# Kernel optimization log

Measured on AMD Instinct MI355X. Metric: run time of the kernel, lower is better.

## Reference

```python
import jax, jax.numpy as jnp
import numpy as np

NGRID = 40
NTOKEN = NGRID * NGRID          # 1600
FEAT = 128
DK = 64
HEAD = 8
NLAYER = 4
EPS = 1e-5
DXDY = (1.0 / (NGRID - 1)) ** 2
SDK = 1.0 / np.sqrt(DK)


def _edges():
    g = jnp.linspace(0.0, 1.0, NGRID)
    gx, gy = jnp.meshgrid(g, g, indexing='ij')
    grid = jnp.stack([gx, gy], axis=-1).reshape(NTOKEN, 2)          # (T,2)
    gi = jnp.broadcast_to(grid[:, None, :], (NTOKEN, NTOKEN, 2))
    gj = jnp.broadcast_to(grid[None, :, :], (NTOKEN, NTOKEN, 2))
    return jnp.concatenate([gi, gj], axis=-1).reshape(NTOKEN * NTOKEN, 4)


def _mlp(x, W1, b1, W2, b2, W3, b3):
    # DenseNet([4,32,64,1], LeakyReLU): activation between layers, none after last
    h = jax.nn.leaky_relu(x @ W1 + b1)
    h = jax.nn.leaky_relu(h @ W2 + b2)
    return h @ W3 + b3


def setup_inputs() -> dict:
    key = jax.random.key(0)
    ks = jax.random.split(key, 24)
    d = {}
    d['xy'] = jax.random.normal(ks[0], (8, 2 * NTOKEN, FEAT), dtype=jnp.float32)
    # kernel / kernelf DenseNet params [4,32,64,1]
    def lin(k, fi, fo):
        s = 1.0 / np.sqrt(fi)
        k1, k2 = jax.random.split(k)
        return (jax.random.uniform(k1, (fi, fo), jnp.float32, -s, s),
                jax.random.uniform(k2, (fo,), jnp.float32, -s, s))
    d['kW1'], d['kb1'] = lin(ks[1], 4, 32)
    d['kW2'], d['kb2'] = lin(ks[2], 32, 64)
    d['kW3'], d['kb3'] = lin(ks[3], 64, 1)
    d['fW1'], d['fb1'] = lin(ks[4], 4, 32)
    d['fW2'], d['fb2'] = lin(ks[5], 32, 64)
    d['fW3'], d['fb3'] = lin(ks[6], 64, 1)
    s = 1.0 / np.sqrt(FEAT)
    d['Wq'] = jax.random.uniform(ks[7], (NLAYER, HEAD, FEAT, DK), jnp.float32, -s, s)
    d['bq'] = jax.random.uniform(ks[8], (NLAYER, HEAD, DK), jnp.float32, -s, s)
    d['Wk'] = jax.random.uniform(ks[9], (NLAYER, HEAD, FEAT, DK), jnp.float32, -s, s)
    d['bk'] = jax.random.uniform(ks[10], (NLAYER, HEAD, DK), jnp.float32, -s, s)
    d['g0'] = jnp.ones((2 * NTOKEN, FEAT), jnp.float32)
    d['b0'] = jnp.zeros((2 * NTOKEN, FEAT), jnp.float32)
    d['gl'] = jnp.ones((NLAYER - 1, FEAT), jnp.float32)
    d['bl'] = jnp.zeros((NLAYER - 1, FEAT), jnp.float32)
    return d


def reference(xy, kW1, kb1, kW2, kb2, kW3, kb3, fW1, fb1, fW2, fb2, fW3, fb3,
              Wq, bq, Wk, bk, g0, b0, gl, bl):
    edges = _edges()                                                   # (T*T,4)
    weight = _mlp(edges, kW1, kb1, kW2, kb2, kW3, kb3).reshape(NTOKEN, NTOKEN)
    weightf = _mlp(edges, fW1, fb1, fW2, fb2, fW3, fb3).reshape(NTOKEN, NTOKEN)
    W2 = jnp.concatenate([weight, weightf], axis=-1)                   # (T, 2T)

    # fcn[0]: LayerNorm over last two dims [2T, F]
    mu = jnp.mean(xy, axis=(1, 2), keepdims=True)
    var = jnp.var(xy, axis=(1, 2), keepdims=True)
    V = (xy - mu) * jax.lax.rsqrt(var + EPS) * g0 + b0                 # (B,2T,F)

    scale = DXDY * SDK
    for j in range(NLAYER - 1):
        Q = jnp.einsum('btf,hfd->bhtd', V, Wq[j]) + bq[j][None, :, None, :]
        K = jnp.einsum('btf,hfd->bhtd', V, Wk[j]) + bk[j][None, :, None, :]
        KV = jnp.einsum('bhtd,btf->bhdf', K, V) * scale                # (B,H,dk,F)
        mid = jnp.einsum('bhtd,bhdf->btf', Q, KV)                      # sum over heads
        m = jnp.mean(mid, axis=-1, keepdims=True)
        v = jnp.var(mid, axis=-1, keepdims=True)
        V = (mid - m) * jax.lax.rsqrt(v + EPS) * gl[j] + bl[j] + V

    j = NLAYER - 1
    Q = jnp.einsum('btf,hfd->bhtd', V, Wq[j]) + bq[j][None, :, None, :]
    K = jnp.einsum('btf,hfd->bhtd', V, Wk[j]) + bk[j][None, :, None, :]
    KV = jnp.einsum('bhtd,btf->bhdf', K[:, :, :NTOKEN, :], xy[:, :NTOKEN, :]) * scale
    out = DXDY * jnp.einsum('nm,bhmd,bhdf->bnf', W2, Q, KV)            # (B,T,F)
    return out
```

## Files before the change

### kernel.cpp

```cpp
#include <hip/hip_runtime.h>
#include <math.h>

#define NGRID 40
#define NT    1600
#define T2    3200
#define F     128
#define NB    8
#define EPS   1e-5f

__device__ __constant__ const float kINV39 = 1.0f/39.0f;
constexpr float DXDY  = (1.0f/39.0f)*(1.0f/39.0f);
constexpr float SCALE = DXDY * 0.125f;

typedef __attribute__((ext_vector_type(8))) short bf16x8;
typedef __attribute__((ext_vector_type(4))) float f32x4;
typedef __attribute__((ext_vector_type(4))) unsigned uint4v;

__device__ __forceinline__ unsigned bitu(float f){ return __builtin_bit_cast(unsigned,f); }
__device__ __forceinline__ float bitf(unsigned u){ return __builtin_bit_cast(float,u); }
__device__ __forceinline__ unsigned short f2bf(float f) {
    unsigned u = bitu(f);
    unsigned r = u + 0x7FFFu + ((u >> 16) & 1u);
    return (unsigned short)(r >> 16);
}
__device__ __forceinline__ float bf2f(unsigned short h) { return bitf(((unsigned)h) << 16); }

__device__ __forceinline__ void pack_hl(float a, float b, unsigned &h, unsigned &l) {
    unsigned ua = bitu(a), ub = bitu(b);
    h = __builtin_amdgcn_perm(ub, ua, 0x07060302u);
    float ra = a - bitf(ua & 0xffff0000u);
    float rb = b - bitf(ub & 0xffff0000u);
    l = __builtin_amdgcn_perm(bitu(rb), bitu(ra), 0x07060302u);
}
__device__ __forceinline__ void store8u(short* dst, const unsigned* p) {
    uint4v v0 = {p[0], p[1], p[2], p[3]};
    uint4v v1 = {p[4], p[5], p[6], p[7]};
    *(uint4v*)dst = v0;
    *(uint4v*)(dst + 8) = v1;
}
__device__ __forceinline__ void store16u(short* dst, const unsigned* p) {
    store8u(dst, p);
    store8u(dst + 16, p + 8);
}

__global__ __launch_bounds__(512) void k_prep_frag(
    const float* __restrict__ kW2, const float* __restrict__ fW2,
    short* __restrict__ Ah, short* __restrict__ Al)
{
    int tid = threadIdx.x;
    int wid = tid >> 6, lane = tid & 63;
    int mlp = wid >> 2, oc = wid & 3;
    const float* W2 = mlp ? fW2 : kW2;
    int row = lane & 15;
    int k0 = (lane >> 4) * 8;
    #pragma unroll
    for (int i = 0; i < 8; ++i) {
        float w = W2[(size_t)(k0 + i) * 64 + oc * 16 + row];
        unsigned short h = f2bf(w);
        Ah[((mlp*4 + oc)*64 + lane)*8 + i] = (short)h;
        Al[((mlp*4 + oc)*64 + lane)*8 + i] = (short)f2bf(w - bf2f(h));
    }
}

__global__ __launch_bounds__(256) void k_prep_uv(
    const float* __restrict__ kW1, const float* __restrict__ kb1,
    const float* __restrict__ fW1, const float* __restrict__ fb1,
    float* __restrict__ uv)
{
    int idx = blockIdx.x * 256 + threadIdx.x;
    int node = idx >> 5, o = idx & 31;
    float x0 = (float)(node / NGRID) * kINV39;
    float x1 = (float)(node % NGRID) * kINV39;
    uv[idx]          = fmaf(kW1[o], x0, fmaf(kW1[32+o], x1, kb1[o]));
    uv[51200 + idx]  = fmaf(kW1[64+o], x0, kW1[96+o]*x1);
    uv[102400 + idx] = fmaf(fW1[o], x0, fmaf(fW1[32+o], x1, fb1[o]));
    uv[153600 + idx] = fmaf(fW1[64+o], x0, fW1[96+o]*x1);
}

#define MLPGRID 1536
__global__ __launch_bounds__(256, 2) void k_mlp_mfma(
    const float* __restrict__ uv,
    const float* __restrict__ kb2, const float* __restrict__ kW3,
    const float* __restrict__ kb3,
    const float* __restrict__ fb2, const float* __restrict__ fW3,
    const float* __restrict__ fb3,
    const short* __restrict__ Ah, const short* __restrict__ Al,
    short* __restrict__ W2h)
{
    int tid = threadIdx.x;
    int wid = tid >> 6, lane = tid & 63;
    int c = lane & 15, kg = lane >> 4;
    int k0 = kg * 8;

    bf16x8 AHf[2][4], ALf[2][4];
    float4 B2f[2][4], W3f[2][4];
    #pragma unroll
    for (int mlp = 0; mlp < 2; ++mlp) {
        const float* b2p = mlp ? fb2 : kb2;
        const float* w3p = mlp ? fW3 : kW3;
        #pragma unroll
        for (int oc = 0; oc < 4; ++oc) {
            AHf[mlp][oc] = *(const bf16x8*)&Ah[((mlp*4 + oc)*64 + lane)*8];
            ALf[mlp][oc] = *(const bf16x8*)&Al[((mlp*4 + oc)*64 + lane)*8];
            B2f[mlp][oc] = *(const float4*)&b2p[oc*16 + kg*4];
            W3f[mlp][oc] = *(const float4*)&w3p[oc*16 + kg*4];
        }
    }
    float bias0 = kb3[0], bias1 = fb3[0];

    int tile = blockIdx.x*4 + wid;
    int n = tile / 100;
    int mt = tile - n*100;
    while (tile < 160000) {
        int m = mt*16 + c;
        float res0, res1;
        #pragma unroll
        for (int mlp = 0; mlp < 2; ++mlp) {
            const float* up = uv + mlp*102400 + n*32 + k0;
            const float* vp = uv + mlp*102400 + 51200 + m*32 + k0;
            float4 ua = *(const float4*)up;
            float4 ub = *(const float4*)(up + 4);
            float4 va = *(const float4*)vp;
            float4 vb = *(const float4*)(vp + 4);
            float h[8] = {ua.x+va.x, ua.y+va.y, ua.z+va.z, ua.w+va.w,
                          ub.x+vb.x, ub.y+vb.y, ub.z+vb.z, ub.w+vb.w};
            #pragma unroll
            for (int i = 0; i < 8; ++i) h[i] = fmaxf(h[i], 0.01f*h[i]);
            unsigned bhp[4], blp[4];
            #pragma unroll
            for (int p = 0; p < 4; ++p)
                pack_hl(h[2*p], h[2*p+1], bhp[p], blp[p]);
            uint4v bhv = {bhp[0], bhp[1], bhp[2], bhp[3]};
            uint4v blv = {blp[0], blp[1], blp[2], blp[3]};
            bf16x8 bh = __builtin_bit_cast(bf16x8, bhv);
            bf16x8 bl = __builtin_bit_cast(bf16x8, blv);
            float acc = 0.f;
            #pragma unroll
            for (int oc = 0; oc < 4; ++oc) {
                f32x4 d = {B2f[mlp][oc].x, B2f[mlp][oc].y,
                           B2f[mlp][oc].z, B2f[mlp][oc].w};
                d = __builtin_amdgcn_mfma_f32_16x16x32_bf16(AHf[mlp][oc], bh, d, 0, 0, 0);
                d = __builtin_amdgcn_mfma_f32_16x16x32_bf16(ALf[mlp][oc], bh, d, 0, 0, 0);
                d = __builtin_amdgcn_mfma_f32_16x16x32_bf16(AHf[mlp][oc], bl, d, 0, 0, 0);
                float w3v[4] = {W3f[mlp][oc].x, W3f[mlp][oc].y,
                                W3f[mlp][oc].z, W3f[mlp][oc].w};
                #pragma unroll
                for (int r = 0; r < 4; ++r)
                    acc = fmaf(fmaxf(d[r], 0.01f*d[r]), w3v[r], acc);
            }
            if (mlp == 0) res0 = acc; else res1 = acc;
        }
        res0 += __shfl_xor(res0, 16); res0 += __shfl_xor(res0, 32);
        res1 += __shfl_xor(res1, 16); res1 += __shfl_xor(res1, 32);
        if (lane < 16) {
            W2h[(size_t)n*T2 + m]      = (short)f2bf(res0 + bias0);
            W2h[(size_t)n*T2 + NT + m] = (short)f2bf(res1 + bias1);
        }
        tile += MLPGRID*4;
        n += 61; mt += 44;
        if (mt >= 100) { mt -= 100; ++n; }
    }
}

__global__ __launch_bounds__(256) void k_precompute_P(
    const float* __restrict__ Wq, const float* __restrict__ bq,
    const float* __restrict__ Wk, const float* __restrict__ bk,
    short* __restrict__ Pnh, short* __restrict__ Pnl,
    float* __restrict__ uB, float* __restrict__ wB, float* __restrict__ cB)
{
    int j = blockIdx.x;
    int part = blockIdx.y;
    const float* wq = Wq + (size_t)j*8*F*64;
    const float* wk = Wk + (size_t)j*8*F*64;
    int tid = threadIdx.x;
    if (part == 8) {
        const float* bqj = bq + j*512;
        const float* bkj = bk + j*512;
        if (tid < 128) {
            int k = tid; float a = 0.f;
            for (int h = 0; h < 8; ++h)
                for (int d = 0; d < 64; ++d)
                    a = fmaf(wq[((size_t)h*F + k)*64 + d], bkj[h*64 + d], a);
            uB[j*128 + k] = a;
        } else {
            int k = tid - 128; float a = 0.f;
            for (int h = 0; h < 8; ++h)
                for (int d = 0; d < 64; ++d)
                    a = fmaf(wk[((size_t)h*F + k)*64 + d], bqj[h*64 + d], a);
            wB[j*128 + k] = a;
        }
        if (tid == 0) {
            float a = 0.f;
            for (int i = 0; i < 512; ++i) a = fmaf(bqj[i], bkj[i], a);
            cB[j] = a;
        }
        return;
    }
    int kp = part*16 + (tid >> 4);
    int k0 = (tid & 15) * 8;
    float acc[8] = {0,0,0,0,0,0,0,0};
    for (int h = 0; h < 8; ++h) {
        const float* wkrow = wk + ((size_t)h*F + kp)*64;
        for (int d = 0; d < 64; ++d) {
            float bv = wkrow[d];
            #pragma unroll
            for (int i = 0; i < 8; ++i)
                acc[i] = fmaf(wq[((size_t)h*F + k0 + i)*64 + d], bv, acc[i]);
        }
    }
    #pragma unroll
    for (int i = 0; i < 8; ++i) {
        float val = acc[i];
        short hs = (short)(bitu(val) >> 16);
        float rem = val - bitf(bitu(val) & 0xffff0000u);
        short ls = (short)(bitu(rem) >> 16);
        Pnh[((size_t)j*128 + k0 + i)*128 + kp] = hs;
        Pnl[((size_t)j*128 + k0 + i)*128 + kp] = ls;
    }
}

__global__ __launch_bounds__(256) void k_ln0_part(
    const float* __restrict__ xy, float* __restrict__ part)
{
    int b = blockIdx.x, blk = blockIdx.y;
    const float4* p = (const float4*)xy + (size_t)b*102400 + blk*4096 + threadIdx.x;
    float s = 0.f, q = 0.f;
    #pragma unroll
    for (int i = 0; i < 16; ++i) {
        float4 v = p[i*256];
        s += (v.x + v.y) + (v.z + v.w);
        q += (v.x*v.x + v.y*v.y) + (v.z*v.z + v.w*v.w);
    }
    #pragma unroll
    for (int off = 32; off >= 1; off >>= 1) {
        s += __shfl_xor(s, off);
        q += __shfl_xor(q, off);
    }
    __shared__ float ss[4], qs[4];
    int wid = threadIdx.x >> 6;
    if ((threadIdx.x & 63) == 0) { ss[wid] = s; qs[wid] = q; }
    __syncthreads();
    if (threadIdx.x == 0) {
        part[((size_t)b*25 + blk)*2 + 0] = ss[0]+ss[1]+ss[2]+ss[3];
        part[((size_t)b*25 + blk)*2 + 1] = qs[0]+qs[1]+qs[2]+qs[3];
    }
}

__global__ void k_ln0_stats(const float* __restrict__ part, float* __restrict__ stats)
{
    int b = threadIdx.x;
    if (b < NB) {
        float s = 0.f, q = 0.f;
        for (int i = 0; i < 25; ++i) {
            s += part[((size_t)b*25 + i)*2 + 0];
            q += part[((size_t)b*25 + i)*2 + 1];
        }
        float mu  = s * (1.0f/409600.0f);
        float var = q * (1.0f/409600.0f) - mu*mu;
        stats[b*2 + 0] = mu;
        stats[b*2 + 1] = rsqrtf(var + EPS);
    }
}

__global__ __launch_bounds__(256) void k_ln0_apply(
    const float* __restrict__ xy, const float* __restrict__ g0,
    const float* __restrict__ b0, const float* __restrict__ stats,
    short* __restrict__ Vbh, short* __restrict__ Vbl,
    short* __restrict__ Vbth, short* __restrict__ Vbtl,
    float* __restrict__ spartV)
{
    int tgrp = blockIdx.x, b = blockIdx.y;
    float mu = stats[b*2], rs = stats[b*2+1];
    __shared__ float T[64][132];
    int tid = threadIdx.x;
    int r = tid >> 2, q = tid & 3;
    int f2 = tid >> 1, half = tid & 1;
    #pragma unroll
    for (int p = 0; p < 2; ++p) {
        int t0 = tgrp*128 + p*64;
        {
            int t = t0 + r;
            const float* xp = xy + ((size_t)b*T2 + t)*F + q*32;
            const float* gp = g0 + (size_t)t*F + q*32;
            const float* bp = b0 + (size_t)t*F + q*32;
            unsigned ph[16], pl[16];
            #pragma unroll
            for (int i = 0; i < 32; i += 4) {
                float4 x = *(const float4*)&xp[i];
                float4 g = *(const float4*)&gp[i];
                float4 bb = *(const float4*)&bp[i];
                float o0 = (x.x - mu)*rs*g.x + bb.x;
                float o1 = (x.y - mu)*rs*g.y + bb.y;
                float o2 = (x.z - mu)*rs*g.z + bb.z;
                float o3 = (x.w - mu)*rs*g.w + bb.w;
                T[r][q*32+i] = o0; T[r][q*32+i+1] = o1;
                T[r][q*32+i+2] = o2; T[r][q*32+i+3] = o3;
                pack_hl(o0, o1, ph[i>>1], pl[i>>1]);
                pack_hl(o2, o3, ph[(i>>1)+1], pl[(i>>1)+1]);
            }
            size_t ob = ((size_t)b*T2 + t)*F + q*32;
            store16u(&Vbh[ob], ph);
            store16u(&Vbl[ob], pl);
        }
        __syncthreads();
        {
            float sacc = 0.f;
            unsigned ph[16], pl[16];
            #pragma unroll
            for (int i = 0; i < 32; i += 2) {
                float v0 = T[half*32 + i][f2];
                float v1 = T[half*32 + i + 1][f2];
                sacc += v0 + v1;
                pack_hl(v0, v1, ph[i>>1], pl[i>>1]);
            }
            size_t ob = ((size_t)b*F + f2)*T2 + t0 + half*32;
            store16u(&Vbth[ob], ph);
            store16u(&Vbtl[ob], pl);
            spartV[((size_t)b*100 + (tgrp*2+p)*2 + half)*128 + f2] = sacc;
        }
        __syncthreads();
    }
}

__global__ __launch_bounds__(256) void k_prep_xyt(
    const float* __restrict__ xy,
    short* __restrict__ xyTh, short* __restrict__ xyTl,
    float* __restrict__ s2part)
{
    int tgrp = blockIdx.x, b = blockIdx.y;
    __shared__ float T[64][132];
    int tid = threadIdx.x;
    int r = tid >> 2, q = tid & 3;
    int f2 = tid >> 1, half = tid & 1;
    int t0 = tgrp*64;
    {
        const float* xp = xy + ((size_t)b*T2 + t0 + r)*F + q*32;
        #pragma unroll
        for (int i = 0; i < 32; i += 4)
            *(float4*)&T[r][q*32+i] = *(const float4*)&xp[i];
    }
    __syncthreads();
    {
        float sacc = 0.f;
        unsigned ph[16], pl[16];
        #pragma unroll
        for (int i = 0; i < 32; i += 2) {
            float v0 = T[half*32 + i][f2];
            float v1 = T[half*32 + i + 1][f2];
            sacc += v0 + v1;
            pack_hl(v0, v1, ph[i>>1], pl[i>>1]);
        }
        size_t ob = ((size_t)b*F + f2)*1600 + t0 + half*32;
        store16u(&xyTh[ob], ph);
        store16u(&xyTl[ob], pl);
        s2part[((size_t)b*50 + tgrp*2 + half)*128 + f2] = sacc;
    }
}

__global__ __launch_bounds__(256) void k_gemm_g_sym(
    const short* __restrict__ Xh, const short* __restrict__ Xl,
    float* __restrict__ Gpart)
{
    int split = blockIdx.x, b = blockIdx.y;
    int t0 = split*128;
    __shared__ __align__(16) short Sh[2][128][40], Sl[2][128][40];
    int tid = threadIdx.x;
    int lane = tid & 63, wid = tid >> 6;
    int wr = wid >> 1, wc = wid & 1;
    int r16 = lane & 15, kg = lane >> 4;
    int sf = tid >> 1, th = tid & 1;

    const short* ph_ = Xh + ((size_t)b*F + sf)*T2 + t0 + th*16;
    const short* pl_ = Xl + ((size_t)b*F + sf)*T2 + t0 + th*16;

    f32x4 acc[4][4];
    #pragma unroll
    for (int i = 0; i < 4; ++i)
        #pragma unroll
        for (int j2 = 0; j2 < 4; ++j2)
            acc[i][j2] = (f32x4){0.f,0.f,0.f,0.f};

    {
        uint4v h0 = *(const uint4v*)ph_,      h1 = *(const uint4v*)(ph_ + 8);
        uint4v l0 = *(const uint4v*)pl_,      l1 = *(const uint4v*)(pl_ + 8);
        *(uint4v*)&Sh[0][sf][th*16]     = h0; *(uint4v*)&Sh[0][sf][th*16+8] = h1;
        *(uint4v*)&Sl[0][sf][th*16]     = l0; *(uint4v*)&Sl[0][sf][th*16+8] = l1;
    }
    #pragma unroll
    for (int ks = 0; ks < 4; ++ks) {
        int cur = ks & 1;
        uint4v h0, h1, l0, l1;
        if (ks < 3) {
            int ko = (ks+1)*32;
            h0 = *(const uint4v*)(ph_ + ko); h1 = *(const uint4v*)(ph_ + ko + 8);
            l0 = *(const uint4v*)(pl_ + ko); l1 = *(const uint4v*)(pl_ + ko + 8);
        }
        __syncthreads();
        bf16x8 ah[4], al[4], bh[4], bl[4];
        #pragma unroll
        for (int i = 0; i < 4; ++i) {
            ah[i] = *(const bf16x8*)&Sh[cur][wr*64 + i*16 + r16][kg*8];
            al[i] = *(const bf16x8*)&Sl[cur][wr*64 + i*16 + r16][kg*8];
            bh[i] = *(const bf16x8*)&Sh[cur][wc*64 + i*16 + r16][kg*8];
            bl[i] = *(const bf16x8*)&Sl[cur][wc*64 + i*16 + r16][kg*8];
        }
        #pragma unroll
        for (int i = 0; i < 4; ++i)
            #pragma unroll
            for (int j2 = 0; j2 < 4; ++j2) {
                acc[i][j2] = __builtin_amdgcn_mfma_f32_16x16x32_bf16(ah[i], bh[j2], acc[i][j2], 0,0,0);
                acc[i][j2] = __builtin_amdgcn_mfma_f32_16x16x32_bf16(al[i], bh[j2], acc[i][j2], 0,0,0);
                acc[i][j2] = __builtin_amdgcn_mfma_f32_16x16x32_bf16(ah[i], bl[j2], acc[i][j2], 0,0,0);
            }
        if (ks < 3) {
            int nb = cur ^ 1;
            *(uint4v*)&Sh[nb][sf][th*16]     = h0; *(uint4v*)&Sh[nb][sf][th*16+8] = h1;
            *(uint4v*)&Sl[nb][sf][th*16]     = l0; *(uint4v*)&Sl[nb][sf][th*16+8] = l1;
        }
    }
    size_t gb = ((size_t)b*25 + split)*16384;
    #pragma unroll
    for (int i = 0; i < 4; ++i)
        #pragma unroll
        for (int j2 = 0; j2 < 4; ++j2)
            #pragma unroll
            for (int reg = 0; reg < 4; ++reg)
                Gpart[gb + (size_t)(wr*64 + i*16 + kg*4 + reg)*128 + wc*64 + j2*16 + r16]
                    = acc[i][j2][reg];
}

__global__ __launch_bounds__(256) void k_gemm_g_asym(
    const short* __restrict__ Ah_, const short* __restrict__ Al_,
    const short* __restrict__ Bh_, const short* __restrict__ Bl_,
    float* __restrict__ Gpart)
{
    int split = blockIdx.x, b = blockIdx.y;
    int t0 = split*64;
    __shared__ __align__(16) short Ahs[128][40], Als[128][40], Bhs[128][40], Bls[128][40];
    int tid = threadIdx.x;
    int lane = tid & 63, wid = tid >> 6;
    int wr = wid >> 1, wc = wid & 1;
    int r16 = lane & 15, kg = lane >> 4;
    int sf = tid >> 1, th = tid & 1;

    const short* pah = Ah_ + ((size_t)b*F + sf)*1600 + t0 + th*16;
    const short* pal = Al_ + ((size_t)b*F + sf)*1600 + t0 + th*16;
    const short* pbh = Bh_ + ((size_t)b*F + sf)*T2   + t0 + th*16;
    const short* pbl = Bl_ + ((size_t)b*F + sf)*T2   + t0 + th*16;

    f32x4 acc[4][4];
    #pragma unroll
    for (int i = 0; i < 4; ++i)
        #pragma unroll
        for (int j2 = 0; j2 < 4; ++j2)
            acc[i][j2] = (f32x4){0.f,0.f,0.f,0.f};

    #pragma unroll
    for (int ks = 0; ks < 2; ++ks) {
        int ko = ks*32;
        if (ks) __syncthreads();
        *(uint4v*)&Ahs[sf][th*16]   = *(const uint4v*)(pah + ko);
        *(uint4v*)&Ahs[sf][th*16+8] = *(const uint4v*)(pah + ko + 8);
        *(uint4v*)&Als[sf][th*16]   = *(const uint4v*)(pal + ko);
        *(uint4v*)&Als[sf][th*16+8] = *(const uint4v*)(pal + ko + 8);
        *(uint4v*)&Bhs[sf][th*16]   = *(const uint4v*)(pbh + ko);
        *(uint4v*)&Bhs[sf][th*16+8] = *(const uint4v*)(pbh + ko + 8);
        *(uint4v*)&Bls[sf][th*16]   = *(const uint4v*)(pbl + ko);
        *(uint4v*)&Bls[sf][th*16+8] = *(const uint4v*)(pbl + ko + 8);
        __syncthreads();
        bf16x8 ah[4], al[4], bh[4], bl[4];
        #pragma unroll
        for (int i = 0; i < 4; ++i) {
            ah[i] = *(const bf16x8*)&Ahs[wr*64 + i*16 + r16][kg*8];
            al[i] = *(const bf16x8*)&Als[wr*64 + i*16 + r16][kg*8];
            bh[i] = *(const bf16x8*)&Bhs[wc*64 + i*16 + r16][kg*8];
            bl[i] = *(const bf16x8*)&Bls[wc*64 + i*16 + r16][kg*8];
        }
        #pragma unroll
        for (int i = 0; i < 4; ++i)
            #pragma unroll
            for (int j2 = 0; j2 < 4; ++j2) {
                acc[i][j2] = __builtin_amdgcn_mfma_f32_16x16x32_bf16(ah[i], bh[j2], acc[i][j2], 0,0,0);
                acc[i][j2] = __builtin_amdgcn_mfma_f32_16x16x32_bf16(al[i], bh[j2], acc[i][j2], 0,0,0);
                acc[i][j2] = __builtin_amdgcn_mfma_f32_16x16x32_bf16(ah[i], bl[j2], acc[i][j2], 0,0,0);
            }
    }
    size_t gb = ((size_t)b*25 + split)*16384;
    #pragma unroll
    for (int i = 0; i < 4; ++i)
        #pragma unroll
        for (int j2 = 0; j2 < 4; ++j2)
            #pragma unroll
            for (int reg = 0; reg < 4; ++reg)
                Gpart[gb + (size_t)(wr*64 + i*16 + kg*4 + reg)*128 + wc*64 + j2*16 + r16]
                    = acc[i][j2][reg];
}

__global__ __launch_bounds__(256) void k_gred(
    const float* __restrict__ Gpart, const float* __restrict__ wj,
    short* __restrict__ Gbh, short* __restrict__ Gbl, float* __restrict__ rpart)
{
    int part = blockIdx.x, b = blockIdx.y;
    int tid = threadIdx.x;
    int e0 = part*2048 + tid*8;
    float a[8] = {0,0,0,0,0,0,0,0};
    for (int i = 0; i < 25; ++i) {
        const float* p = Gpart + ((size_t)b*25 + i)*16384 + e0;
        float4 x0 = *(const float4*)p;
        float4 x1 = *(const float4*)(p + 4);
        a[0] += x0.x; a[1] += x0.y; a[2] += x0.z; a[3] += x0.w;
        a[4] += x1.x; a[5] += x1.y; a[6] += x1.z; a[7] += x1.w;
    }
    unsigned ph[4], pl[4];
    #pragma unroll
    for (int i = 0; i < 8; i += 2) pack_hl(a[i], a[i+1], ph[i>>1], pl[i>>1]);
    uint4v vh = {ph[0],ph[1],ph[2],ph[3]};
    uint4v vl = {pl[0],pl[1],pl[2],pl[3]};
    *(uint4v*)&Gbh[(size_t)b*16384 + e0] = vh;
    *(uint4v*)&Gbl[(size_t)b*16384 + e0] = vl;

    int c0 = e0 & 127;
    float4 w0 = *(const float4*)&wj[c0];
    float4 w1 = *(const float4*)&wj[c0 + 4];
    float pr = a[0]*w0.x + a[1]*w0.y + a[2]*w0.z + a[3]*w0.w
             + a[4]*w1.x + a[5]*w1.y + a[6]*w1.z + a[7]*w1.w;
    pr += __shfl_xor(pr, 1); pr += __shfl_xor(pr, 2);
    pr += __shfl_xor(pr, 4); pr += __shfl_xor(pr, 8);
    if ((tid & 15) == 0) rpart[b*128 + (e0 >> 7)] = pr;
}

struct CMStage {
    short Psh[2][64][40], Psl[2][64][40];
    short Bsh[2][128][40], Bsl[2][128][40];
};
__global__ __launch_bounds__(256) void k_computeM(
    const short* __restrict__ Gbh, const short* __restrict__ Gbl,
    const float* __restrict__ spart, int np,
    const short* __restrict__ Pjh, const short* __restrict__ Pjl,
    const float* __restrict__ uj, const float* __restrict__ cj,
    const float* __restrict__ rpart,
    short* __restrict__ Mth, short* __restrict__ Mtl, float* __restrict__ rm)
{
    int kh = blockIdx.x, b = blockIdx.y;
    __shared__ __align__(16) char smem[sizeof(CMStage)];
    CMStage& S = *(CMStage*)smem;
    float (*T)[132] = (float(*)[132])smem;
    __shared__ float sv[128];

    int tid = threadIdx.x;
    int lane = tid & 63, wid = tid >> 6;
    int wr = wid >> 1, wc = wid & 1;
    int r16 = lane & 15, kg = lane >> 4;
    int st = tid >> 2, sq = tid & 3;
    int sf = tid >> 1, sh2 = tid & 1;

    if (tid < 128) {
        float s = 0.f;
        for (int i = 0; i < np; ++i) s += spart[((size_t)b*np + i)*128 + tid];
        sv[tid] = s;
        if (kh == 0) rm[b*128 + tid] = SCALE*(rpart[b*128 + tid] + cj[0]*s);
    }

    const short* pah = Pjh + (size_t)(kh*64 + st)*128 + sq*8;
    const short* pal = Pjl + (size_t)(kh*64 + st)*128 + sq*8;
    const short* pbh = Gbh + ((size_t)b*F + sf)*128 + sh2*16;
    const short* pbl = Gbl + ((size_t)b*F + sf)*128 + sh2*16;

    f32x4 acc[2][4];
    #pragma unroll
    for (int i = 0; i < 2; ++i)
        #pragma unroll
        for (int j2 = 0; j2 < 4; ++j2)
            acc[i][j2] = (f32x4){0.f,0.f,0.f,0.f};

    {
        *(uint4v*)&S.Psh[0][st][sq*8]      = *(const uint4v*)pah;
        *(uint4v*)&S.Psl[0][st][sq*8]      = *(const uint4v*)pal;
        *(uint4v*)&S.Bsh[0][sf][sh2*16]    = *(const uint4v*)pbh;
        *(uint4v*)&S.Bsh[0][sf][sh2*16+8]  = *(const uint4v*)(pbh + 8);
        *(uint4v*)&S.Bsl[0][sf][sh2*16]    = *(const uint4v*)pbl;
        *(uint4v*)&S.Bsl[0][sf][sh2*16+8]  = *(const uint4v*)(pbl + 8);
    }
    #pragma unroll
    for (int ks = 0; ks < 4; ++ks) {
        int cur = ks & 1;
        uint4v a0, a1, b0, b1, b2, b3;
        if (ks < 3) {
            int ko = (ks+1)*32;
            a0 = *(const uint4v*)(pah + ko); a1 = *(const uint4v*)(pal + ko);
            b0 = *(const uint4v*)(pbh + ko); b1 = *(const uint4v*)(pbh + ko + 8);
            b2 = *(const uint4v*)(pbl + ko); b3 = *(const uint4v*)(pbl + ko + 8);
        }
        __syncthreads();
        bf16x8 ah[2], al[2], bh[4], bl[4];
        #pragma unroll
        for (int i = 0; i < 2; ++i) {
            ah[i] = *(const bf16x8*)&S.Psh[cur][wr*32 + i*16 + r16][kg*8];
            al[i] = *(const bf16x8*)&S.Psl[cur][wr*32 + i*16 + r16][kg*8];
        }
        #pragma unroll
        for (int j2 = 0; j2 < 4; ++j2) {
            bh[j2] = *(const bf16x8*)&S.Bsh[cur][wc*64 + j2*16 + r16][kg*8];
            bl[j2] = *(const bf16x8*)&S.Bsl[cur][wc*64 + j2*16 + r16][kg*8];
        }
        #pragma unroll
        for (int i = 0; i < 2; ++i)
            #pragma unroll
            for (int j2 = 0; j2 < 4; ++j2) {
                acc[i][j2] = __builtin_amdgcn_mfma_f32_16x16x32_bf16(ah[i], bh[j2], acc[i][j2], 0,0,0);
                acc[i][j2] = __builtin_amdgcn_mfma_f32_16x16x32_bf16(al[i], bh[j2], acc[i][j2], 0,0,0);
                acc[i][j2] = __builtin_amdgcn_mfma_f32_16x16x32_bf16(ah[i], bl[j2], acc[i][j2], 0,0,0);
            }
        if (ks < 3) {
            int nb = cur ^ 1;
            *(uint4v*)&S.Psh[nb][st][sq*8]     = a0;
            *(uint4v*)&S.Psl[nb][st][sq*8]     = a1;
            *(uint4v*)&S.Bsh[nb][sf][sh2*16]   = b0;
            *(uint4v*)&S.Bsh[nb][sf][sh2*16+8] = b1;
            *(uint4v*)&S.Bsl[nb][sf][sh2*16]   = b2;
            *(uint4v*)&S.Bsl[nb][sf][sh2*16+8] = b3;
        }
    }
    float uval[2][4], svv[4];
    #pragma unroll
    for (int i = 0; i < 2; ++i)
        #pragma unroll
        for (int reg = 0; reg < 4; ++reg)
            uval[i][reg] = uj[kh*64 + wr*32 + i*16 + kg*4 + reg];
    #pragma unroll
    for (int j2 = 0; j2 < 4; ++j2) svv[j2] = sv[wc*64 + j2*16 + r16];
    __syncthreads();
    #pragma unroll
    for (int i = 0; i < 2; ++i)
        #pragma unroll
        for (int j2 = 0; j2 < 4; ++j2)
            #pragma unroll
            for (int reg = 0; reg < 4; ++reg)
                T[wr*32 + i*16 + kg*4 + reg][wc*64 + j2*16 + r16]
                    = SCALE*(acc[i][j2][reg] + uval[i][reg]*svv[j2]);
    __syncthreads();
    {
        int f2 = tid >> 1, half = tid & 1;
        unsigned ph[16], pl[16];
        #pragma unroll
        for (int i = 0; i < 32; i += 2) {
            float v0 = T[half*32 + i][f2];
            float v1 = T[half*32 + i + 1][f2];
            pack_hl(v0, v1, ph[i>>1], pl[i>>1]);
        }
        size_t ob = ((size_t)b*F + f2)*F + kh*64 + half*32;
        store16u(&Mth[ob], ph);
        store16u(&Mtl[ob], pl);
    }
}

struct MidStage {
    short Ash[2][64][40], Asl[2][64][40];
    short Bsh[2][128][40], Bsl[2][128][40];
};
__global__ __launch_bounds__(256) void k_mid(
    short* __restrict__ Vbh, short* __restrict__ Vbl,
    const short* __restrict__ Mth, const short* __restrict__ Mtl,
    const float* __restrict__ rm,
    const float* __restrict__ glj, const float* __restrict__ blj, int doLN,
    short* __restrict__ OTh, short* __restrict__ OTl,
    float* __restrict__ spartN)
{
    int tblk = blockIdx.x, b = blockIdx.y;
    int t0 = tblk * 64;
    __shared__ __align__(16) char smem[sizeof(MidStage)];
    MidStage& S = *(MidStage*)smem;
    float (*T)[132] = (float(*)[132])smem;

    int tid = threadIdx.x;
    int lane = tid & 63, wid = tid >> 6;
    int wr = wid >> 1, wc = wid & 1;
    int r16 = lane & 15, kg = lane >> 4;
    int st = tid >> 2, sq = tid & 3;
    int sf = tid >> 1, sh2 = tid & 1;

    const short* pah = Vbh + ((size_t)b*T2 + t0 + st)*F + sq*8;
    const short* pal = Vbl + ((size_t)b*T2 + t0 + st)*F + sq*8;
    const short* pbh = Mth + ((size_t)b*F + sf)*F + sh2*16;
    const short* pbl = Mtl + ((size_t)b*F + sf)*F + sh2*16;

    f32x4 acc[2][4];
    #pragma unroll
    for (int i = 0; i < 2; ++i)
        #pragma unroll
        for (int j2 = 0; j2 < 4; ++j2)
            acc[i][j2] = (f32x4){0.f,0.f,0.f,0.f};

    {
        *(uint4v*)&S.Ash[0][st][sq*8]      = *(const uint4v*)pah;
        *(uint4v*)&S.Asl[0][st][sq*8]      = *(const uint4v*)pal;
        *(uint4v*)&S.Bsh[0][sf][sh2*16]    = *(const uint4v*)pbh;
        *(uint4v*)&S.Bsh[0][sf][sh2*16+8]  = *(const uint4v*)(pbh + 8);
        *(uint4v*)&S.Bsl[0][sf][sh2*16]    = *(const uint4v*)pbl;
        *(uint4v*)&S.Bsl[0][sf][sh2*16+8]  = *(const uint4v*)(pbl + 8);
    }
    #pragma unroll
    for (int ks = 0; ks < 4; ++ks) {
        int cur = ks & 1;
        uint4v a0, a1, b0, b1, b2, b3;
        if (ks < 3) {
            int ko = (ks+1)*32;
            a0 = *(const uint4v*)(pah + ko); a1 = *(const uint4v*)(pal + ko);
            b0 = *(const uint4v*)(pbh + ko); b1 = *(const uint4v*)(pbh + ko + 8);
            b2 = *(const uint4v*)(pbl + ko); b3 = *(const uint4v*)(pbl + ko + 8);
        }
        __syncthreads();
        bf16x8 ah[2], al[2], bh[4], bl[4];
        #pragma unroll
        for (int i = 0; i < 2; ++i) {
            ah[i] = *(const bf16x8*)&S.Ash[cur][wr*32 + i*16 + r16][kg*8];
            al[i] = *(const bf16x8*)&S.Asl[cur][wr*32 + i*16 + r16][kg*8];
        }
        #pragma unroll
        for (int j2 = 0; j2 < 4; ++j2) {
            bh[j2] = *(const bf16x8*)&S.Bsh[cur][wc*64 + j2*16 + r16][kg*8];
            bl[j2] = *(const bf16x8*)&S.Bsl[cur][wc*64 + j2*16 + r16][kg*8];
        }
        #pragma unroll
        for (int i = 0; i < 2; ++i)
            #pragma unroll
            for (int j2 = 0; j2 < 4; ++j2) {
                acc[i][j2] = __builtin_amdgcn_mfma_f32_16x16x32_bf16(ah[i], bh[j2], acc[i][j2], 0,0,0);
                acc[i][j2] = __builtin_amdgcn_mfma_f32_16x16x32_bf16(al[i], bh[j2], acc[i][j2], 0,0,0);
                acc[i][j2] = __builtin_amdgcn_mfma_f32_16x16x32_bf16(ah[i], bl[j2], acc[i][j2], 0,0,0);
            }
        if (ks < 3) {
            int nb = cur ^ 1;
            *(uint4v*)&S.Ash[nb][st][sq*8]     = a0;
            *(uint4v*)&S.Asl[nb][st][sq*8]     = a1;
            *(uint4v*)&S.Bsh[nb][sf][sh2*16]   = b0;
            *(uint4v*)&S.Bsh[nb][sf][sh2*16+8] = b1;
            *(uint4v*)&S.Bsl[nb][sf][sh2*16]   = b2;
            *(uint4v*)&S.Bsl[nb][sf][sh2*16+8] = b3;
        }
    }
    float rv[4];
    #pragma unroll
    for (int j2 = 0; j2 < 4; ++j2) rv[j2] = rm[b*F + wc*64 + j2*16 + r16];
    __syncthreads();
    #pragma unroll
    for (int i = 0; i < 2; ++i)
        #pragma unroll
        for (int j2 = 0; j2 < 4; ++j2)
            #pragma unroll
            for (int reg = 0; reg < 4; ++reg)
                T[wr*32 + i*16 + kg*4 + reg][wc*64 + j2*16 + r16]
                    = acc[i][j2][reg] + rv[j2];
    __syncthreads();

    if (doLN) {
        int r = tid >> 2, q = tid & 3;
        float v[32];
        #pragma unroll
        for (int i = 0; i < 32; i += 4)
            *(float4*)&v[i] = *(const float4*)&T[r][q*32 + i];
        float s = 0.f;
        #pragma unroll
        for (int i = 0; i < 32; ++i) s += v[i];
        s += __shfl_xor(s, 1); s += __shfl_xor(s, 2);
        float mu = s * (1.0f/128.0f);
        float dv = 0.f;
        #pragma unroll
        for (int i = 0; i < 32; ++i) { float d = v[i] - mu; dv = fmaf(d, d, dv); }
        dv += __shfl_xor(dv, 1); dv += __shfl_xor(dv, 2);
        float rs = rsqrtf(dv * (1.0f/128.0f) + EPS);

        short hb[32], lb[32];
        {
            const short* rh = Vbh + ((size_t)b*T2 + t0 + r)*F + q*32;
            const short* rl = Vbl + ((size_t)b*T2 + t0 + r)*F + q*32;
            #pragma unroll
            for (int i = 0; i < 32; i += 8) {
                *(uint4v*)&hb[i] = *(const uint4v*)(rh + i);
                *(uint4v*)&lb[i] = *(const uint4v*)(rl + i);
            }
        }
        float gv[32], bv2[32];
        #pragma unroll
        for (int i = 0; i < 32; i += 4) {
            *(float4*)&gv[i]  = *(const float4*)&glj[q*32 + i];
            *(float4*)&bv2[i] = *(const float4*)&blj[q*32 + i];
        }
        unsigned ph[16], pl[16];
        #pragma unroll
        for (int i = 0; i < 32; i += 2) {
            float res0 = bf2f((unsigned short)hb[i])   + bf2f((unsigned short)lb[i]);
            float res1 = bf2f((unsigned short)hb[i+1]) + bf2f((unsigned short)lb[i+1]);
            float o0 = (v[i]   - mu)*rs*gv[i]   + bv2[i]   + res0;
            float o1 = (v[i+1] - mu)*rs*gv[i+1] + bv2[i+1] + res1;
            T[r][q*32+i] = o0; T[r][q*32+i+1] = o1;
            pack_hl(o0, o1, ph[i>>1], pl[i>>1]);
        }
        size_t ob = ((size_t)b*T2 + t0 + r)*F + q*32;
        store16u(&Vbh[ob], ph);
        store16u(&Vbl[ob], pl);
        __syncthreads();
    }
    {
        int f2 = tid >> 1, half = tid & 1;
        float sacc = 0.f;
        unsigned ph[16], pl[16];
        #pragma unroll
        for (int i = 0; i < 32; i += 2) {
            float v0 = T[half*32 + i][f2];
            float v1 = T[half*32 + i + 1][f2];
            sacc += v0 + v1;
            pack_hl(v0, v1, ph[i>>1], pl[i>>1]);
        }
        size_t ob = ((size_t)b*F + f2)*T2 + t0 + half*32;
        store16u(&OTh[ob], ph);
        store16u(&OTl[ob], pl);
        if (doLN)
            spartN[((size_t)b*100 + tblk*2 + half)*128 + f2] = sacc;
    }
}

__global__ __launch_bounds__(256) void k_gemm_out_mfma(
    const short* __restrict__ W2h,
    const short* __restrict__ Uth, const short* __restrict__ Utl,
    float* __restrict__ out)
{
    int id = blockIdx.x;
    int qb = id >> 3;
    if (qb >= 25) return;
    int job = (id & 7) * 25 + qb;
    int nt = job >> 3, b = job & 7;
    int n0 = nt * 64;

    __shared__ __align__(16) short As[2][64][40];
    __shared__ __align__(16) short Bh_s[2][128][40], Bl_s[2][128][40];

    int tid = threadIdx.x;
    int lane = tid & 63, wid = tid >> 6;
    int wr = wid >> 1, wc = wid & 1;
    int r16 = lane & 15, kg = lane >> 4;
    int srow = tid >> 2, sq2 = tid & 3;
    int sf = tid >> 1, sh2 = tid & 1;

    const short* ap  = W2h + (size_t)(n0 + srow)*T2 + sq2*8;
    const short* bhp = Uth + ((size_t)b*F + sf)*T2 + sh2*16;
    const short* blp = Utl + ((size_t)b*F + sf)*T2 + sh2*16;

    f32x4 acc[2][4];
    #pragma unroll
    for (int i = 0; i < 2; ++i)
        #pragma unroll
        for (int j2 = 0; j2 < 4; ++j2)
            acc[i][j2] = (f32x4){0.f,0.f,0.f,0.f};

    {
        *(uint4v*)&As[0][srow][sq2*8]     = *(const uint4v*)ap;
        *(uint4v*)&Bh_s[0][sf][sh2*16]    = *(const uint4v*)bhp;
        *(uint4v*)&Bh_s[0][sf][sh2*16+8]  = *(const uint4v*)(bhp + 8);
        *(uint4v*)&Bl_s[0][sf][sh2*16]    = *(const uint4v*)blp;
        *(uint4v*)&Bl_s[0][sf][sh2*16+8]  = *(const uint4v*)(blp + 8);
    }
    for (int it = 0; it < 100; ++it) {
        int cur = it & 1;
        uint4v ra, b0, b1, b2, b3;
        if (it < 99) {
            int ko = (it + 1) * 32;
            ra = *(const uint4v*)(ap + ko);
            b0 = *(const uint4v*)(bhp + ko); b1 = *(const uint4v*)(bhp + ko + 8);
            b2 = *(const uint4v*)(blp + ko); b3 = *(const uint4v*)(blp + ko + 8);
        }
        __syncthreads();
        bf16x8 ah[2], bh[4], bl[4];
        #pragma unroll
        for (int i = 0; i < 2; ++i)
            ah[i] = *(const bf16x8*)&As[cur][wr*32 + i*16 + r16][kg*8];
        #pragma unroll
        for (int j2 = 0; j2 < 4; ++j2) {
            bh[j2] = *(const bf16x8*)&Bh_s[cur][wc*64 + j2*16 + r16][kg*8];
            bl[j2] = *(const bf16x8*)&Bl_s[cur][wc*64 + j2*16 + r16][kg*8];
        }
        #pragma unroll
        for (int i = 0; i < 2; ++i)
            #pragma unroll
            for (int j2 = 0; j2 < 4; ++j2) {
                acc[i][j2] = __builtin_amdgcn_mfma_f32_16x16x32_bf16(ah[i], bh[j2], acc[i][j2], 0,0,0);
                acc[i][j2] = __builtin_amdgcn_mfma_f32_16x16x32_bf16(ah[i], bl[j2], acc[i][j2], 0,0,0);
            }
        if (it < 99) {
            int nb = cur ^ 1;
            *(uint4v*)&As[nb][srow][sq2*8]    = ra;
            *(uint4v*)&Bh_s[nb][sf][sh2*16]   = b0;
            *(uint4v*)&Bh_s[nb][sf][sh2*16+8] = b1;
            *(uint4v*)&Bl_s[nb][sf][sh2*16]   = b2;
            *(uint4v*)&Bl_s[nb][sf][sh2*16+8] = b3;
        }
    }
    #pragma unroll
    for (int i = 0; i < 2; ++i)
        #pragma unroll
        for (int j2 = 0; j2 < 4; ++j2)
            #pragma unroll
            for (int reg = 0; reg < 4; ++reg) {
                int n_out = n0 + wr*32 + i*16 + kg*4 + reg;
                int f_out = wc*64 + j2*16 + r16;
                out[((size_t)b*NT + n_out)*F + f_out] = DXDY * acc[i][j2][reg];
            }
}

extern "C" void kernel_launch(void* const* d_in, const int* in_sizes, int n_in,
                              void* d_out, int out_size, void* d_ws, size_t ws_size,
                              hipStream_t stream)
{
    const float* xy  = (const float*)d_in[0];
    const float* kW1 = (const float*)d_in[1];
    const float* kb1 = (const float*)d_in[2];
    const float* kW2 = (const float*)d_in[3];
    const float* kb2 = (const float*)d_in[4];
    const float* kW3 = (const float*)d_in[5];
    const float* kb3 = (const float*)d_in[6];
    const float* fW1 = (const float*)d_in[7];
    const float* fb1 = (const float*)d_in[8];
    const float* fW2 = (const float*)d_in[9];
    const float* fb2 = (const float*)d_in[10];
    const float* fW3 = (const float*)d_in[11];
    const float* fb3 = (const float*)d_in[12];
    const float* Wq  = (const float*)d_in[13];
    const float* bq  = (const float*)d_in[14];
    const float* Wk  = (const float*)d_in[15];
    const float* bk  = (const float*)d_in[16];
    const float* g0  = (const float*)d_in[17];
    const float* b0  = (const float*)d_in[18];
    const float* gl  = (const float*)d_in[19];
    const float* bl  = (const float*)d_in[20];
    float* out = (float*)d_out;

    short* W2h  = (short*)d_ws;
    short* Vbh  = W2h  + 5120000;
    short* Vbl  = Vbh  + 3276800;
    short* Vbth = Vbl  + 3276800;
    short* Vbtl = Vbth + 3276800;
    short* xyTh = Vbtl + 3276800;
    short* xyTl = xyTh + 1638400;
    short* Uth  = xyTl + 1638400;
    short* Utl  = Uth  + 3276800;
    short* Pnh  = Utl  + 3276800;
    short* Pnl  = Pnh  + 65536;
    short* Mth  = Pnl  + 65536;
    short* Mtl  = Mth  + 131072;
    short* Gbh  = Mtl  + 131072;
    short* Gbl  = Gbh  + 131072;
    short* AhF  = Gbl  + 131072;
    short* AlF  = AhF  + 4096;
    float* Gpart  = (float*)(AlF + 4096);
    float* uB     = Gpart + 3276800;
    float* wB     = uB + 512;
    float* cB     = wB + 512;
    float* lnpart = cB + 4;
    float* lnstats= lnpart + 400;
    float* rpart  = lnstats + 16;
    float* rm     = rpart + 1024;
    float* spartV = rm + 1024;
    float* s2part = spartV + 102400;
    float* uvT    = s2part + 51200;

    k_prep_frag<<<1, 512, 0, stream>>>(kW2, fW2, AhF, AlF);
    k_prep_uv<<<dim3(200), 256, 0, stream>>>(kW1, kb1, fW1, fb1, uvT);
    k_mlp_mfma<<<dim3(MLPGRID), 256, 0, stream>>>(uvT, kb2, kW3, kb3,
                                                  fb2, fW3, fb3, AhF, AlF, W2h);
    k_precompute_P<<<dim3(4,9), 256, 0, stream>>>(Wq, bq, Wk, bk, Pnh, Pnl, uB, wB, cB);
    k_ln0_part<<<dim3(8,25), 256, 0, stream>>>(xy, lnpart);
    k_ln0_stats<<<1, 64, 0, stream>>>(lnpart, lnstats);
    k_ln0_apply<<<dim3(25,8), 256, 0, stream>>>(xy, g0, b0, lnstats,
                                                Vbh, Vbl, Vbth, Vbtl, spartV);
    k_prep_xyt<<<dim3(25,8), 256, 0, stream>>>(xy, xyTh, xyTl, s2part);

    for (int j = 0; j < 4; ++j) {
        if (j < 3)
            k_gemm_g_sym<<<dim3(25,8), 256, 0, stream>>>(Vbth, Vbtl, Gpart);
        else
            k_gemm_g_asym<<<dim3(25,8), 256, 0, stream>>>(xyTh, xyTl, Vbth, Vbtl, Gpart);
        k_gred<<<dim3(8,8), 256, 0, stream>>>(Gpart, wB + j*128, Gbh, Gbl, rpart);
        k_computeM<<<dim3(2,8), 256, 0, stream>>>(
            Gbh, Gbl,
            (j < 3) ? spartV : s2part, (j < 3) ? 100 : 50,
            Pnh + (size_t)j*16384, Pnl + (size_t)j*16384,
            uB + j*128, cB + j, rpart, Mth, Mtl, rm);
        if (j < 3)
            k_mid<<<dim3(50,8), 256, 0, stream>>>(Vbh, Vbl, Mth, Mtl, rm,
                                                  gl + j*128, bl + j*128, 1,
                                                  Vbth, Vbtl, spartV);
        else
            k_mid<<<dim3(50,8), 256, 0, stream>>>(Vbh, Vbl, Mth, Mtl, rm,
                                                  gl, bl, 0,
                                                  Uth, Utl, spartV);
    }

    k_gemm_out_mfma<<<dim3(256), 256, 0, stream>>>(W2h, Uth, Utl, out);
}
```

Baseline: 548.5 us.

## Merge prep kernels and run layer loop as one cooperative persistent kernel

Several small setup kernels (uv prep, LN partial sums, P precompute, W2 fragment prep) are merged into one launch, and the LN stats kernel is removed by having each apply block reduce the partials itself. The whole per-layer chain (gemm G, reduce, computeM, mid, final output GEMM) now runs inside a single cooperative kernel that uses grid.sync between stages, removing about twenty kernel launches and their gaps. If the cooperative launch fails, the code falls back to separate wrapper kernels. The cost is grid-wide barriers with many blocks idle in the small stages, a shared-memory union sized for the largest stage, and the output GEMM now running on 200 blocks instead of 256.

```diff
diff --git a/kernel.cpp b/kernel.cpp
--- a/kernel.cpp
+++ b/kernel.cpp
@@ -1,5 +1,8 @@
 #include <hip/hip_runtime.h>
+#include <hip/hip_cooperative_groups.h>
 #include <math.h>
+
+namespace cg = cooperative_groups;
 
 #define NGRID 40
 #define NT    1600
@@ -43,38 +46,124 @@
     store8u(dst + 16, p + 8);
 }
 
-__global__ __launch_bounds__(512) void k_prep_frag(
+__global__ __launch_bounds__(256) void k_prep(
     const float* __restrict__ kW2, const float* __restrict__ fW2,
-    short* __restrict__ Ah, short* __restrict__ Al)
-{
-    int tid = threadIdx.x;
-    int wid = tid >> 6, lane = tid & 63;
-    int mlp = wid >> 2, oc = wid & 3;
-    const float* W2 = mlp ? fW2 : kW2;
-    int row = lane & 15;
-    int k0 = (lane >> 4) * 8;
-    #pragma unroll
-    for (int i = 0; i < 8; ++i) {
-        float w = W2[(size_t)(k0 + i) * 64 + oc * 16 + row];
-        unsigned short h = f2bf(w);
-        Ah[((mlp*4 + oc)*64 + lane)*8 + i] = (short)h;
-        Al[((mlp*4 + oc)*64 + lane)*8 + i] = (short)f2bf(w - bf2f(h));
-    }
-}
-
-__global__ __launch_bounds__(256) void k_prep_uv(
+    short* __restrict__ Ah, short* __restrict__ Al,
     const float* __restrict__ kW1, const float* __restrict__ kb1,
     const float* __restrict__ fW1, const float* __restrict__ fb1,
-    float* __restrict__ uv)
-{
-    int idx = blockIdx.x * 256 + threadIdx.x;
-    int node = idx >> 5, o = idx & 31;
-    float x0 = (float)(node / NGRID) * kINV39;
-    float x1 = (float)(node % NGRID) * kINV39;
-    uv[idx]          = fmaf(kW1[o], x0, fmaf(kW1[32+o], x1, kb1[o]));
-    uv[51200 + idx]  = fmaf(kW1[64+o], x0, kW1[96+o]*x1);
-    uv[102400 + idx] = fmaf(fW1[o], x0, fmaf(fW1[32+o], x1, fb1[o]));
-    uv[153600 + idx] = fmaf(fW1[64+o], x0, fW1[96+o]*x1);
+    float* __restrict__ uv,
+    const float* __restrict__ xy, float* __restrict__ lnpart,
+    const float* __restrict__ Wq, const float* __restrict__ bq,
+    const float* __restrict__ Wk, const float* __restrict__ bk,
+    short* __restrict__ Pnh, short* __restrict__ Pnl,
+    float* __restrict__ uB, float* __restrict__ wB, float* __restrict__ cB)
+{
+    __shared__ float ss[4], qs[4];
+    int job = blockIdx.x;
+    int tid = threadIdx.x;
+    if (job < 200) {
+        int idx = job * 256 + tid;
+        int node = idx >> 5, o = idx & 31;
+        float x0 = (float)(node / NGRID) * kINV39;
+        float x1 = (float)(node % NGRID) * kINV39;
+        uv[idx]          = fmaf(kW1[o], x0, fmaf(kW1[32+o], x1, kb1[o]));
+        uv[51200 + idx]  = fmaf(kW1[64+o], x0, kW1[96+o]*x1);
+        uv[102400 + idx] = fmaf(fW1[o], x0, fmaf(fW1[32+o], x1, fb1[o]));
+        uv[153600 + idx] = fmaf(fW1[64+o], x0, fW1[96+o]*x1);
+        return;
+    }
+    if (job < 400) {
+        int t = job - 200;
+        int b = t & 7, blk = t >> 3;
+        const float4* p = (const float4*)xy + (size_t)b*102400 + blk*4096 + tid;
+        float s = 0.f, q = 0.f;
+        #pragma unroll
+        for (int i = 0; i < 16; ++i) {
+            float4 v = p[i*256];
+            s += (v.x + v.y) + (v.z + v.w);
+            q += (v.x*v.x + v.y*v.y) + (v.z*v.z + v.w*v.w);
+        }
+        #pragma unroll
+        for (int off = 32; off >= 1; off >>= 1) {
+            s += __shfl_xor(s, off);
+            q += __shfl_xor(q, off);
+        }
+        int wid = tid >> 6;
+        if ((tid & 63) == 0) { ss[wid] = s; qs[wid] = q; }
+        __syncthreads();
+        if (tid == 0) {
+            lnpart[((size_t)b*25 + blk)*2 + 0] = ss[0]+ss[1]+ss[2]+ss[3];
+            lnpart[((size_t)b*25 + blk)*2 + 1] = qs[0]+qs[1]+qs[2]+qs[3];
+        }
+        return;
+    }
+    if (job < 436) {
+        int t = job - 400;
+        int j = t & 3, part = t >> 2;
+        const float* wq = Wq + (size_t)j*8*F*64;
+        const float* wk = Wk + (size_t)j*8*F*64;
+        if (part == 8) {
+            const float* bqj = bq + j*512;
+            const float* bkj = bk + j*512;
+            if (tid < 128) {
+                int k = tid; float a = 0.f;
+                for (int h = 0; h < 8; ++h)
+                    for (int d = 0; d < 64; ++d)
+                        a = fmaf(wq[((size_t)h*F + k)*64 + d], bkj[h*64 + d], a);
+                uB[j*128 + k] = a;
+            } else {
+                int k = tid - 128; float a = 0.f;
+                for (int h = 0; h < 8; ++h)
+                    for (int d = 0; d < 64; ++d)
+                        a = fmaf(wk[((size_t)h*F + k)*64 + d], bqj[h*64 + d], a);
+                wB[j*128 + k] = a;
+            }
+            if (tid == 0) {
+                float a = 0.f;
+                for (int i = 0; i < 512; ++i) a = fmaf(bqj[i], bkj[i], a);
+                cB[j] = a;
+            }
+            return;
+        }
+        int kp = part*16 + (tid >> 4);
+        int k0 = (tid & 15) * 8;
+        float acc[8] = {0,0,0,0,0,0,0,0};
+        for (int h = 0; h < 8; ++h) {
+            const float* wkrow = wk + ((size_t)h*F + kp)*64;
+            for (int d = 0; d < 64; ++d) {
+                float bv = wkrow[d];
+                #pragma unroll
+                for (int i = 0; i < 8; ++i)
+                    acc[i] = fmaf(wq[((size_t)h*F + k0 + i)*64 + d], bv, acc[i]);
+            }
+        }
+        #pragma unroll
+        for (int i = 0; i < 8; ++i) {
+            float val = acc[i];
+            short hs = (short)(bitu(val) >> 16);
+            float rem = val - bitf(bitu(val) & 0xffff0000u);
+            short ls = (short)(bitu(rem) >> 16);
+            Pnh[((size_t)j*128 + k0 + i)*128 + kp] = hs;
+            Pnl[((size_t)j*128 + k0 + i)*128 + kp] = ls;
+        }
+        return;
+    }
+    {
+        int oc = tid >> 6, lane = tid & 63;
+        int row = lane & 15;
+        int k0 = (lane >> 4) * 8;
+        #pragma unroll
+        for (int mlp = 0; mlp < 2; ++mlp) {
+            const float* W2 = mlp ? fW2 : kW2;
+            #pragma unroll
+            for (int i = 0; i < 8; ++i) {
+                float w = W2[(size_t)(k0 + i) * 64 + oc * 16 + row];
+                unsigned short h = f2bf(w);
+                Ah[((mlp*4 + oc)*64 + lane)*8 + i] = (short)h;
+                Al[((mlp*4 + oc)*64 + lane)*8 + i] = (short)f2bf(w - bf2f(h));
+            }
+        }
+    }
 }
 
 #define MLPGRID 1536
@@ -162,127 +251,43 @@
     }
 }
 
-__global__ __launch_bounds__(256) void k_precompute_P(
-    const float* __restrict__ Wq, const float* __restrict__ bq,
-    const float* __restrict__ Wk, const float* __restrict__ bk,
-    short* __restrict__ Pnh, short* __restrict__ Pnl,
-    float* __restrict__ uB, float* __restrict__ wB, float* __restrict__ cB)
-{
-    int j = blockIdx.x;
-    int part = blockIdx.y;
-    const float* wq = Wq + (size_t)j*8*F*64;
-    const float* wk = Wk + (size_t)j*8*F*64;
-    int tid = threadIdx.x;
-    if (part == 8) {
-        const float* bqj = bq + j*512;
-        const float* bkj = bk + j*512;
-        if (tid < 128) {
-            int k = tid; float a = 0.f;
-            for (int h = 0; h < 8; ++h)
-                for (int d = 0; d < 64; ++d)
-                    a = fmaf(wq[((size_t)h*F + k)*64 + d], bkj[h*64 + d], a);
-            uB[j*128 + k] = a;
-        } else {
-            int k = tid - 128; float a = 0.f;
-            for (int h = 0; h < 8; ++h)
-                for (int d = 0; d < 64; ++d)
-                    a = fmaf(wk[((size_t)h*F + k)*64 + d], bqj[h*64 + d], a);
-            wB[j*128 + k] = a;
-        }
-        if (tid == 0) {
-            float a = 0.f;
-            for (int i = 0; i < 512; ++i) a = fmaf(bqj[i], bkj[i], a);
-            cB[j] = a;
-        }
-        return;
-    }
-    int kp = part*16 + (tid >> 4);
-    int k0 = (tid & 15) * 8;
-    float acc[8] = {0,0,0,0,0,0,0,0};
-    for (int h = 0; h < 8; ++h) {
-        const float* wkrow = wk + ((size_t)h*F + kp)*64;
-        for (int d = 0; d < 64; ++d) {
-            float bv = wkrow[d];
-            #pragma unroll
-            for (int i = 0; i < 8; ++i)
-                acc[i] = fmaf(wq[((size_t)h*F + k0 + i)*64 + d], bv, acc[i]);
-        }
-    }
-    #pragma unroll
-    for (int i = 0; i < 8; ++i) {
-        float val = acc[i];
-        short hs = (short)(bitu(val) >> 16);
-        float rem = val - bitf(bitu(val) & 0xffff0000u);
-        short ls = (short)(bitu(rem) >> 16);
-        Pnh[((size_t)j*128 + k0 + i)*128 + kp] = hs;
-        Pnl[((size_t)j*128 + k0 + i)*128 + kp] = ls;
-    }
-}
-
-__global__ __launch_bounds__(256) void k_ln0_part(
-    const float* __restrict__ xy, float* __restrict__ part)
-{
-    int b = blockIdx.x, blk = blockIdx.y;
-    const float4* p = (const float4*)xy + (size_t)b*102400 + blk*4096 + threadIdx.x;
-    float s = 0.f, q = 0.f;
-    #pragma unroll
-    for (int i = 0; i < 16; ++i) {
-        float4 v = p[i*256];
-        s += (v.x + v.y) + (v.z + v.w);
-        q += (v.x*v.x + v.y*v.y) + (v.z*v.z + v.w*v.w);
-    }
-    #pragma unroll
-    for (int off = 32; off >= 1; off >>= 1) {
-        s += __shfl_xor(s, off);
-        q += __shfl_xor(q, off);
-    }
-    __shared__ float ss[4], qs[4];
-    int wid = threadIdx.x >> 6;
-    if ((threadIdx.x & 63) == 0) { ss[wid] = s; qs[wid] = q; }
-    __syncthreads();
-    if (threadIdx.x == 0) {
-        part[((size_t)b*25 + blk)*2 + 0] = ss[0]+ss[1]+ss[2]+ss[3];
-        part[((size_t)b*25 + blk)*2 + 1] = qs[0]+qs[1]+qs[2]+qs[3];
-    }
-}
-
-__global__ void k_ln0_stats(const float* __restrict__ part, float* __restrict__ stats)
-{
-    int b = threadIdx.x;
-    if (b < NB) {
-        float s = 0.f, q = 0.f;
-        for (int i = 0; i < 25; ++i) {
-            s += part[((size_t)b*25 + i)*2 + 0];
-            q += part[((size_t)b*25 + i)*2 + 1];
-        }
-        float mu  = s * (1.0f/409600.0f);
-        float var = q * (1.0f/409600.0f) - mu*mu;
-        stats[b*2 + 0] = mu;
-        stats[b*2 + 1] = rsqrtf(var + EPS);
-    }
-}
-
-__global__ __launch_bounds__(256) void k_ln0_apply(
+struct SMem {
+    __align__(16) char buf[61440];
+    float sv[128];
+};
+struct GSymS  { short Sh[2][128][40], Sl[2][128][40]; };
+struct GAsymS { short Ahs[128][40], Als[128][40], Bhs[128][40], Bls[128][40]; };
+struct CMS    { short Psh[2][64][40], Psl[2][64][40], Bsh[2][128][40], Bsl[2][128][40]; };
+struct MidS   { short Ash[2][64][40], Asl[2][64][40], Bsh[2][128][40], Bsl[2][128][40]; };
+struct GOutS  { short As[2][64][40], Bh[2][128][40], Bl[2][128][40]; };
+
+__device__ void body_apply(int job,
     const float* __restrict__ xy, const float* __restrict__ g0,
-    const float* __restrict__ b0, const float* __restrict__ stats,
+    const float* __restrict__ b0, const float* __restrict__ lnpart,
     short* __restrict__ Vbh, short* __restrict__ Vbl,
     short* __restrict__ Vbth, short* __restrict__ Vbtl,
-    float* __restrict__ spartV)
-{
-    int tgrp = blockIdx.x, b = blockIdx.y;
-    float mu = stats[b*2], rs = stats[b*2+1];
-    __shared__ float T[64][132];
+    float* __restrict__ spartV, SMem& S)
+{
+    int tgrp = job % 25, b = job / 25;
+    float s = 0.f, q = 0.f;
+    for (int i = 0; i < 25; ++i) {
+        s += lnpart[((size_t)b*25 + i)*2 + 0];
+        q += lnpart[((size_t)b*25 + i)*2 + 1];
+    }
+    float mu = s * (1.0f/409600.0f);
+    float rs = rsqrtf(q * (1.0f/409600.0f) - mu*mu + EPS);
+    float (*T)[132] = (float(*)[132])S.buf;
     int tid = threadIdx.x;
-    int r = tid >> 2, q = tid & 3;
+    int r = tid >> 2, qd = tid & 3;
     int f2 = tid >> 1, half = tid & 1;
     #pragma unroll
     for (int p = 0; p < 2; ++p) {
         int t0 = tgrp*128 + p*64;
         {
             int t = t0 + r;
-            const float* xp = xy + ((size_t)b*T2 + t)*F + q*32;
-            const float* gp = g0 + (size_t)t*F + q*32;
-            const float* bp = b0 + (size_t)t*F + q*32;
+            const float* xp = xy + ((size_t)b*T2 + t)*F + qd*32;
+            const float* gp = g0 + (size_t)t*F + qd*32;
+            const float* bp = b0 + (size_t)t*F + qd*32;
             unsigned ph[16], pl[16];
             #pragma unroll
             for (int i = 0; i < 32; i += 4) {
@@ -293,12 +298,12 @@
                 float o1 = (x.y - mu)*rs*g.y + bb.y;
                 float o2 = (x.z - mu)*rs*g.z + bb.z;
                 float o3 = (x.w - mu)*rs*g.w + bb.w;
-                T[r][q*32+i] = o0; T[r][q*32+i+1] = o1;
-                T[r][q*32+i+2] = o2; T[r][q*32+i+3] = o3;
+                T[r][qd*32+i] = o0; T[r][qd*32+i+1] = o1;
+                T[r][qd*32+i+2] = o2; T[r][qd*32+i+3] = o3;
                 pack_hl(o0, o1, ph[i>>1], pl[i>>1]);
                 pack_hl(o2, o3, ph[(i>>1)+1], pl[(i>>1)+1]);
             }
-            size_t ob = ((size_t)b*T2 + t)*F + q*32;
+            size_t ob = ((size_t)b*T2 + t)*F + qd*32;
             store16u(&Vbh[ob], ph);
             store16u(&Vbl[ob], pl);
         }
@@ -322,22 +327,22 @@
     }
 }
 
-__global__ __launch_bounds__(256) void k_prep_xyt(
+__device__ void body_xyt(int job,
     const float* __restrict__ xy,
     short* __restrict__ xyTh, short* __restrict__ xyTl,
-    float* __restrict__ s2part)
-{
-    int tgrp = blockIdx.x, b = blockIdx.y;
-    __shared__ float T[64][132];
+    float* __restrict__ s2part, SMem& S)
+{
+    int tgrp = job % 25, b = job / 25;
+    float (*T)[132] = (float(*)[132])S.buf;
     int tid = threadIdx.x;
-    int r = tid >> 2, q = tid & 3;
+    int r = tid >> 2, qd = tid & 3;
     int f2 = tid >> 1, half = tid & 1;
     int t0 = tgrp*64;
     {
-        const float* xp = xy + ((size_t)b*T2 + t0 + r)*F + q*32;
+        const float* xp = xy + ((size_t)b*T2 + t0 + r)*F + qd*32;
         #pragma unroll
         for (int i = 0; i < 32; i += 4)
-            *(float4*)&T[r][q*32+i] = *(const float4*)&xp[i];
+            *(float4*)&T[r][qd*32+i] = *(const float4*)&xp[i];
     }
     __syncthreads();
     {
@@ -357,13 +362,13 @@
     }
 }
 
-__global__ __launch_bounds__(256) void k_gemm_g_sym(
+__device__ void body_gsym(int job,
     const short* __restrict__ Xh, const short* __restrict__ Xl,
-    float* __restrict__ Gpart)
-{
-    int split = blockIdx.x, b = blockIdx.y;
+    float* __restrict__ Gpart, SMem& Smem)
+{
+    int split = job % 25, b = job / 25;
     int t0 = split*128;
-    __shared__ __align__(16) short Sh[2][128][40], Sl[2][128][40];
+    GSymS& S = *(GSymS*)Smem.buf;
     int tid = threadIdx.x;
     int lane = tid & 63, wid = tid >> 6;
     int wr = wid >> 1, wc = wid & 1;
@@ -383,8 +388,8 @@
     {
         uint4v h0 = *(const uint4v*)ph_,      h1 = *(const uint4v*)(ph_ + 8);
         uint4v l0 = *(const uint4v*)pl_,      l1 = *(const uint4v*)(pl_ + 8);
-        *(uint4v*)&Sh[0][sf][th*16]     = h0; *(uint4v*)&Sh[0][sf][th*16+8] = h1;
-        *(uint4v*)&Sl[0][sf][th*16]     = l0; *(uint4v*)&Sl[0][sf][th*16+8] = l1;
+        *(uint4v*)&S.Sh[0][sf][th*16]     = h0; *(uint4v*)&S.Sh[0][sf][th*16+8] = h1;
+        *(uint4v*)&S.Sl[0][sf][th*16]     = l0; *(uint4v*)&S.Sl[0][sf][th*16+8] = l1;
     }
     #pragma unroll
     for (int ks = 0; ks < 4; ++ks) {
@@ -399,10 +404,10 @@
         bf16x8 ah[4], al[4], bh[4], bl[4];
         #pragma unroll
         for (int i = 0; i < 4; ++i) {
-            ah[i] = *(const bf16x8*)&Sh[cur][wr*64 + i*16 + r16][kg*8];
-            al[i] = *(const bf16x8*)&Sl[cur][wr*64 + i*16 + r16][kg*8];
-            bh[i] = *(const bf16x8*)&Sh[cur][wc*64 + i*16 + r16][kg*8];
-            bl[i] = *(const bf16x8*)&Sl[cur][wc*64 + i*16 + r16][kg*8];
+            ah[i] = *(const bf16x8*)&S.Sh[cur][wr*64 + i*16 + r16][kg*8];
+            al[i] = *(const bf16x8*)&S.Sl[cur][wr*64 + i*16 + r16][kg*8];
+            bh[i] = *(const bf16x8*)&S.Sh[cur][wc*64 + i*16 + r16][kg*8];
+            bl[i] = *(const bf16x8*)&S.Sl[cur][wc*64 + i*16 + r16][kg*8];
         }
         #pragma unroll
         for (int i = 0; i < 4; ++i)
@@ -414,10 +419,11 @@
             }
         if (ks < 3) {
             int nb = cur ^ 1;
-            *(uint4v*)&Sh[nb][sf][th*16]     = h0; *(uint4v*)&Sh[nb][sf][th*16+8] = h1;
-            *(uint4v*)&Sl[nb][sf][th*16]     = l0; *(uint4v*)&Sl[nb][sf][th*16+8] = l1;
-        }
-    }
+            *(uint4v*)&S.Sh[nb][sf][th*16]     = h0; *(uint4v*)&S.Sh[nb][sf][th*16+8] = h1;
+            *(uint4v*)&S.Sl[nb][sf][th*16]     = l0; *(uint4v*)&S.Sl[nb][sf][th*16+8] = l1;
+        }
+    }
+    __syncthreads();
     size_t gb = ((size_t)b*25 + split)*16384;
     #pragma unroll
     for (int i = 0; i < 4; ++i)
@@ -429,14 +435,14 @@
                     = acc[i][j2][reg];
 }
 
-__global__ __launch_bounds__(256) void k_gemm_g_asym(
+__device__ void body_gasym(int job,
     const short* __restrict__ Ah_, const short* __restrict__ Al_,
     const short* __restrict__ Bh_, const short* __restrict__ Bl_,
-    float* __restrict__ Gpart)
-{
-    int split = blockIdx.x, b = blockIdx.y;
+    float* __restrict__ Gpart, SMem& Smem)
+{
+    int split = job % 25, b = job / 25;
     int t0 = split*64;
-    __shared__ __align__(16) short Ahs[128][40], Als[128][40], Bhs[128][40], Bls[128][40];
+    GAsymS& S = *(GAsymS*)Smem.buf;
     int tid = threadIdx.x;
     int lane = tid & 63, wid = tid >> 6;
     int wr = wid >> 1, wc = wid & 1;
@@ -458,23 +464,23 @@
     #pragma unroll
     for (int ks = 0; ks < 2; ++ks) {
         int ko = ks*32;
-        if (ks) __syncthreads();
-        *(uint4v*)&Ahs[sf][th*16]   = *(const uint4v*)(pah + ko);
-        *(uint4v*)&Ahs[sf][th*16+8] = *(const uint4v*)(pah + ko + 8);
-        *(uint4v*)&Als[sf][th*16]   = *(const uint4v*)(pal + ko);
-        *(uint4v*)&Als[sf][th*16+8] = *(const uint4v*)(pal + ko + 8);
-        *(uint4v*)&Bhs[sf][th*16]   = *(const uint4v*)(pbh + ko);
-        *(uint4v*)&Bhs[sf][th*16+8] = *(const uint4v*)(pbh + ko + 8);
-        *(uint4v*)&Bls[sf][th*16]   = *(const uint4v*)(pbl + ko);
-        *(uint4v*)&Bls[sf][th*16+8] = *(const uint4v*)(pbl + ko + 8);
+        __syncthreads();
+        *(uint4v*)&S.Ahs[sf][th*16]   = *(const uint4v*)(pah + ko);
+        *(uint4v*)&S.Ahs[sf][th*16+8] = *(const uint4v*)(pah + ko + 8);
+        *(uint4v*)&S.Als[sf][th*16]   = *(const uint4v*)(pal + ko);
+        *(uint4v*)&S.Als[sf][th*16+8] = *(const uint4v*)(pal + ko + 8);
+        *(uint4v*)&S.Bhs[sf][th*16]   = *(const uint4v*)(pbh + ko);
+        *(uint4v*)&S.Bhs[sf][th*16+8] = *(const uint4v*)(pbh + ko + 8);
+        *(uint4v*)&S.Bls[sf][th*16]   = *(const uint4v*)(pbl + ko);
+        *(uint4v*)&S.Bls[sf][th*16+8] = *(const uint4v*)(pbl + ko + 8);
         __syncthreads();
         bf16x8 ah[4], al[4], bh[4], bl[4];
         #pragma unroll
         for (int i = 0; i < 4; ++i) {
-            ah[i] = *(const bf16x8*)&Ahs[wr*64 + i*16 + r16][kg*8];
-            al[i] = *(const bf16x8*)&Als[wr*64 + i*16 + r16][kg*8];
-            bh[i] = *(const bf16x8*)&Bhs[wc*64 + i*16 + r16][kg*8];
-            bl[i] = *(const bf16x8*)&Bls[wc*64 + i*16 + r16][kg*8];
+            ah[i] = *(const bf16x8*)&S.Ahs[wr*64 + i*16 + r16][kg*8];
+            al[i] = *(const bf16x8*)&S.Als[wr*64 + i*16 + r16][kg*8];
+            bh[i] = *(const bf16x8*)&S.Bhs[wc*64 + i*16 + r16][kg*8];
+            bl[i] = *(const bf16x8*)&S.Bls[wc*64 + i*16 + r16][kg*8];
         }
         #pragma unroll
         for (int i = 0; i < 4; ++i)
@@ -485,6 +491,7 @@
                 acc[i][j2] = __builtin_amdgcn_mfma_f32_16x16x32_bf16(ah[i], bl[j2], acc[i][j2], 0,0,0);
             }
     }
+    __syncthreads();
     size_t gb = ((size_t)b*25 + split)*16384;
     #pragma unroll
     for (int i = 0; i < 4; ++i)
@@ -496,11 +503,11 @@
                     = acc[i][j2][reg];
 }
 
-__global__ __launch_bounds__(256) void k_gred(
+__device__ void body_gred(int job,
     const float* __restrict__ Gpart, const float* __restrict__ wj,
     short* __restrict__ Gbh, short* __restrict__ Gbl, float* __restrict__ rpart)
 {
-    int part = blockIdx.x, b = blockIdx.y;
+    int part = job % 8, b = job / 8;
     int tid = threadIdx.x;
     int e0 = part*2048 + tid*8;
     float a[8] = {0,0,0,0,0,0,0,0};
@@ -529,23 +536,19 @@
     if ((tid & 15) == 0) rpart[b*128 + (e0 >> 7)] = pr;
 }
 
-struct CMStage {
-    short Psh[2][64][40], Psl[2][64][40];
-    short Bsh[2][128][40], Bsl[2][128][40];
-};
-__global__ __launch_bounds__(256) void k_computeM(
+__device__ void body_computeM(int job,
     const short* __restrict__ Gbh, const short* __restrict__ Gbl,
     const float* __restrict__ spart, int np,
     const short* __restrict__ Pjh, const short* __restrict__ Pjl,
     const float* __restrict__ uj, const float* __restrict__ cj,
     const float* __restrict__ rpart,
-    short* __restrict__ Mth, short* __restrict__ Mtl, float* __restrict__ rm)
-{
-    int kh = blockIdx.x, b = blockIdx.y;
-    __shared__ __align__(16) char smem[sizeof(CMStage)];
-    CMStage& S = *(CMStage*)smem;
-    float (*T)[132] = (float(*)[132])smem;
-    __shared__ float sv[128];
+    short* __restrict__ Mth, short* __restrict__ Mtl, float* __restrict__ rm,
+    SMem& Smem)
+{
+    int kh = job % 2, b = job / 2;
+    CMS& S = *(CMS*)Smem.buf;
+    float (*T)[132] = (float(*)[132])Smem.buf;
+    float* sv = Smem.sv;
 
     int tid = threadIdx.x;
     int lane = tid & 63, wid = tid >> 6;
@@ -654,23 +657,18 @@
     }
 }
 
-struct MidStage {
-    short Ash[2][64][40], Asl[2][64][40];
-    short Bsh[2][128][40], Bsl[2][128][40];
-};
-__global__ __launch_bounds__(256) void k_mid(
+__device__ void body_mid(int job,
     short* __restrict__ Vbh, short* __restrict__ Vbl,
     const short* __restrict__ Mth, const short* __restrict__ Mtl,
     const float* __restrict__ rm,
     const float* __restrict__ glj, const float* __restrict__ blj, int doLN,
     short* __restrict__ OTh, short* __restrict__ OTl,
-    float* __restrict__ spartN)
-{
-    int tblk = blockIdx.x, b = blockIdx.y;
+    float* __restrict__ spartN, SMem& Smem)
+{
+    int tblk = job % 50, b = job / 50;
     int t0 = tblk * 64;
-    __shared__ __align__(16) char smem[sizeof(MidStage)];
-    MidStage& S = *(MidStage*)smem;
-    float (*T)[132] = (float(*)[132])smem;
+    MidS& S = *(MidS*)Smem.buf;
+    float (*T)[132] = (float(*)[132])Smem.buf;
 
     int tid = threadIdx.x;
     int lane = tid & 63, wid = tid >> 6;
@@ -754,11 +752,11 @@
     __syncthreads();
 
     if (doLN) {
-        int r = tid >> 2, q = tid & 3;
+        int r = tid >> 2, qd = tid & 3;
         float v[32];
         #pragma unroll
         for (int i = 0; i < 32; i += 4)
-            *(float4*)&v[i] = *(const float4*)&T[r][q*32 + i];
+            *(float4*)&v[i] = *(const float4*)&T[r][qd*32 + i];
         float s = 0.f;
         #pragma unroll
         for (int i = 0; i < 32; ++i) s += v[i];
@@ -772,8 +770,8 @@
 
         short hb[32], lb[32];
         {
-            const short* rh = Vbh + ((size_t)b*T2 + t0 + r)*F + q*32;
-            const short* rl = Vbl + ((size_t)b*T2 + t0 + r)*F + q*32;
+            const short* rh = Vbh + ((size_t)b*T2 + t0 + r)*F + qd*32;
+            const short* rl = Vbl + ((size_t)b*T2 + t0 + r)*F + qd*32;
             #pragma unroll
             for (int i = 0; i < 32; i += 8) {
                 *(uint4v*)&hb[i] = *(const uint4v*)(rh + i);
@@ -783,8 +781,8 @@
         float gv[32], bv2[32];
         #pragma unroll
         for (int i = 0; i < 32; i += 4) {
-            *(float4*)&gv[i]  = *(const float4*)&glj[q*32 + i];
-            *(float4*)&bv2[i] = *(const float4*)&blj[q*32 + i];
+            *(float4*)&gv[i]  = *(const float4*)&glj[qd*32 + i];
+            *(float4*)&bv2[i] = *(const float4*)&blj[qd*32 + i];
         }
         unsigned ph[16], pl[16];
         #pragma unroll
@@ -793,10 +791,10 @@
             float res1 = bf2f((unsigned short)hb[i+1]) + bf2f((unsigned short)lb[i+1]);
             float o0 = (v[i]   - mu)*rs*gv[i]   + bv2[i]   + res0;
             float o1 = (v[i+1] - mu)*rs*gv[i+1] + bv2[i+1] + res1;
-            T[r][q*32+i] = o0; T[r][q*32+i+1] = o1;
+            T[r][qd*32+i] = o0; T[r][qd*32+i+1] = o1;
             pack_hl(o0, o1, ph[i>>1], pl[i>>1]);
         }
-        size_t ob = ((size_t)b*T2 + t0 + r)*F + q*32;
+        size_t ob = ((size_t)b*T2 + t0 + r)*F + qd*32;
         store16u(&Vbh[ob], ph);
         store16u(&Vbl[ob], pl);
         __syncthreads();
@@ -820,20 +818,14 @@
     }
 }
 
-__global__ __launch_bounds__(256) void k_gemm_out_mfma(
+__device__ void body_gout(int job,
     const short* __restrict__ W2h,
     const short* __restrict__ Uth, const short* __restrict__ Utl,
-    float* __restrict__ out)
-{
-    int id = blockIdx.x;
-    int qb = id >> 3;
-    if (qb >= 25) return;
-    int job = (id & 7) * 25 + qb;
-    int nt = job >> 3, b = job & 7;
+    float* __restrict__ out, SMem& Smem)
+{
+    int nt = job % 25, b = job / 25;
     int n0 = nt * 64;
-
-    __shared__ __align__(16) short As[2][64][40];
-    __shared__ __align__(16) short Bh_s[2][128][40], Bl_s[2][128][40];
+    GOutS& S = *(GOutS*)Smem.buf;
 
     int tid = threadIdx.x;
     int lane = tid & 63, wid = tid >> 6;
@@ -854,11 +846,11 @@
             acc[i][j2] = (f32x4){0.f,0.f,0.f,0.f};
 
     {
-        *(uint4v*)&As[0][srow][sq2*8]     = *(const uint4v*)ap;
-        *(uint4v*)&Bh_s[0][sf][sh2*16]    = *(const uint4v*)bhp;
-        *(uint4v*)&Bh_s[0][sf][sh2*16+8]  = *(const uint4v*)(bhp + 8);
-        *(uint4v*)&Bl_s[0][sf][sh2*16]    = *(const uint4v*)blp;
-        *(uint4v*)&Bl_s[0][sf][sh2*16+8]  = *(const uint4v*)(blp + 8);
+        *(uint4v*)&S.As[0][srow][sq2*8]  = *(const uint4v*)ap;
+        *(uint4v*)&S.Bh[0][sf][sh2*16]   = *(const uint4v*)bhp;
+        *(uint4v*)&S.Bh[0][sf][sh2*16+8] = *(const uint4v*)(bhp + 8);
+        *(uint4v*)&S.Bl[0][sf][sh2*16]   = *(const uint4v*)blp;
+        *(uint4v*)&S.Bl[0][sf][sh2*16+8] = *(const uint4v*)(blp + 8);
     }
     for (int it = 0; it < 100; ++it) {
         int cur = it & 1;
@@ -873,11 +865,11 @@
         bf16x8 ah[2], bh[4], bl[4];
         #pragma unroll
         for (int i = 0; i < 2; ++i)
-            ah[i] = *(const bf16x8*)&As[cur][wr*32 + i*16 + r16][kg*8];
+            ah[i] = *(const bf16x8*)&S.As[cur][wr*32 + i*16 + r16][kg*8];
         #pragma unroll
         for (int j2 = 0; j2 < 4; ++j2) {
-            bh[j2] = *(const bf16x8*)&Bh_s[cur][wc*64 + j2*16 + r16][kg*8];
-            bl[j2] = *(const bf16x8*)&Bl_s[cur][wc*64 + j2*16 + r16][kg*8];
+            bh[j2] = *(const bf16x8*)&S.Bh[cur][wc*64 + j2*16 + r16][kg*8];
+            bl[j2] = *(const bf16x8*)&S.Bl[cur][wc*64 + j2*16 + r16][kg*8];
         }
         #pragma unroll
         for (int i = 0; i < 2; ++i)
@@ -888,13 +880,14 @@
             }
         if (it < 99) {
             int nb = cur ^ 1;
-            *(uint4v*)&As[nb][srow][sq2*8]    = ra;
-            *(uint4v*)&Bh_s[nb][sf][sh2*16]   = b0;
-            *(uint4v*)&Bh_s[nb][sf][sh2*16+8] = b1;
-            *(uint4v*)&Bl_s[nb][sf][sh2*16]   = b2;
-            *(uint4v*)&Bl_s[nb][sf][sh2*16+8] = b3;
-        }
-    }
+            *(uint4v*)&S.As[nb][srow][sq2*8]  = ra;
+            *(uint4v*)&S.Bh[nb][sf][sh2*16]   = b0;
+            *(uint4v*)&S.Bh[nb][sf][sh2*16+8] = b1;
+            *(uint4v*)&S.Bl[nb][sf][sh2*16]   = b2;
+            *(uint4v*)&S.Bl[nb][sf][sh2*16+8] = b3;
+        }
+    }
+    __syncthreads();
     #pragma unroll
     for (int i = 0; i < 2; ++i)
         #pragma unroll
@@ -905,6 +898,106 @@
                 int f_out = wc*64 + j2*16 + r16;
                 out[((size_t)b*NT + n_out)*F + f_out] = DXDY * acc[i][j2][reg];
             }
+}
+
+__global__ __launch_bounds__(256) void k_coop(
+    const float* xy, const float* g0, const float* b0,
+    const float* gl, const float* bl, const float* lnpart,
+    short* Vbh, short* Vbl, short* Vbth, short* Vbtl,
+    short* xyTh, short* xyTl, short* Uth, short* Utl,
+    float* spartV, float* s2part, float* Gpart,
+    short* Gbh, short* Gbl, float* rpart, float* rm,
+    short* Mth, short* Mtl, const short* Pnh, const short* Pnl,
+    const float* uB, const float* wB, const float* cB,
+    const short* W2h, float* out)
+{
+    __shared__ SMem S;
+    cg::grid_group grid = cg::this_grid();
+    int bid = blockIdx.x;
+
+    for (int j2 = bid; j2 < 400; j2 += 256) {
+        if (j2 < 200) body_apply(j2, xy, g0, b0, lnpart, Vbh, Vbl, Vbth, Vbtl, spartV, S);
+        else          body_xyt(j2 - 200, xy, xyTh, xyTl, s2part, S);
+        __syncthreads();
+    }
+    grid.sync();
+
+    for (int j = 0; j < 4; ++j) {
+        if (bid < 200) {
+            if (j < 3) body_gsym(bid, Vbth, Vbtl, Gpart, S);
+            else       body_gasym(bid, xyTh, xyTl, Vbth, Vbtl, Gpart, S);
+        }
+        grid.sync();
+        if (bid < 64) body_gred(bid, Gpart, wB + j*128, Gbh, Gbl, rpart);
+        grid.sync();
+        if (bid < 16) body_computeM(bid, Gbh, Gbl,
+                                    (j < 3) ? spartV : s2part, (j < 3) ? 100 : 50,
+                                    Pnh + (size_t)j*16384, Pnl + (size_t)j*16384,
+                                    uB + j*128, cB + j, rpart, Mth, Mtl, rm, S);
+        grid.sync();
+        for (int j2 = bid; j2 < 400; j2 += 256) {
+            if (j < 3) body_mid(j2, Vbh, Vbl, Mth, Mtl, rm, gl + j*128, bl + j*128, 1,
+                                Vbth, Vbtl, spartV, S);
+            else       body_mid(j2, Vbh, Vbl, Mth, Mtl, rm, gl, bl, 0,
+                                Uth, Utl, spartV, S);
+            __syncthreads();
+        }
+        grid.sync();
+    }
+    if (bid < 200) body_gout(bid, W2h, Uth, Utl, out, S);
+}
+
+__global__ __launch_bounds__(256) void k_apply_w(
+    const float* xy, const float* g0, const float* b0, const float* lnpart,
+    short* Vbh, short* Vbl, short* Vbth, short* Vbtl,
+    short* xyTh, short* xyTl, float* spartV, float* s2part)
+{
+    __shared__ SMem S;
+    int jb = blockIdx.x;
+    if (jb < 200) body_apply(jb, xy, g0, b0, lnpart, Vbh, Vbl, Vbth, Vbtl, spartV, S);
+    else          body_xyt(jb - 200, xy, xyTh, xyTl, s2part, S);
+}
+__global__ __launch_bounds__(256) void k_gsym_w(
+    const short* Xh, const short* Xl, float* Gpart)
+{
+    __shared__ SMem S;
+    body_gsym(blockIdx.x, Xh, Xl, Gpart, S);
+}
+__global__ __launch_bounds__(256) void k_gasym_w(
+    const short* Ah_, const short* Al_, const short* Bh_, const short* Bl_,
+    float* Gpart)
+{
+    __shared__ SMem S;
+    body_gasym(blockIdx.x, Ah_, Al_, Bh_, Bl_, Gpart, S);
+}
+__global__ __launch_bounds__(256) void k_gred_w(
+    const float* Gpart, const float* wj, short* Gbh, short* Gbl, float* rpart)
+{
+    body_gred(blockIdx.x, Gpart, wj, Gbh, Gbl, rpart);
+}
+__global__ __launch_bounds__(256) void k_cm_w(
+    const short* Gbh, const short* Gbl, const float* spart, int np,
+    const short* Pjh, const short* Pjl, const float* uj, const float* cj,
+    const float* rpart, short* Mth, short* Mtl, float* rm)
+{
+    __shared__ SMem S;
+    body_computeM(blockIdx.x, Gbh, Gbl, spart, np, Pjh, Pjl, uj, cj, rpart,
+                  Mth, Mtl, rm, S);
+}
+__global__ __launch_bounds__(256) void k_mid_w(
+    short* Vbh, short* Vbl, const short* Mth, const short* Mtl,
+    const float* rm, const float* glj, const float* blj, int doLN,
+    short* OTh, short* OTl, float* spartN)
+{
+    __shared__ SMem S;
+    body_mid(blockIdx.x, Vbh, Vbl, Mth, Mtl, rm, glj, blj, doLN, OTh, OTl,
+             spartN, S);
+}
+__global__ __launch_bounds__(256) void k_gout_w(
+    const short* W2h, const short* Uth, const short* Utl, float* out)
+{
+    __shared__ SMem S;
+    body_gout(blockIdx.x, W2h, Uth, Utl, out, S);
 }
 
 extern "C" void kernel_launch(void* const* d_in, const int* in_sizes, int n_in,
@@ -956,44 +1049,57 @@
     float* wB     = uB + 512;
     float* cB     = wB + 512;
     float* lnpart = cB + 4;
-    float* lnstats= lnpart + 400;
-    float* rpart  = lnstats + 16;
+    float* rpart  = lnpart + 400;
     float* rm     = rpart + 1024;
     float* spartV = rm + 1024;
     float* s2part = spartV + 102400;
     float* uvT    = s2part + 51200;
 
-    k_prep_frag<<<1, 512, 0, stream>>>(kW2, fW2, AhF, AlF);
-    k_prep_uv<<<dim3(200), 256, 0, stream>>>(kW1, kb1, fW1, fb1, uvT);
+    k_prep<<<dim3(437), 256, 0, stream>>>(kW2, fW2, AhF, AlF,
+                                          kW1, kb1, fW1, fb1, uvT,
+                                          xy, lnpart,
+                                          Wq, bq, Wk, bk, Pnh, Pnl, uB, wB, cB);
+
     k_mlp_mfma<<<dim3(MLPGRID), 256, 0, stream>>>(uvT, kb2, kW3, kb3,
                                                   fb2, fW3, fb3, AhF, AlF, W2h);
-    k_precompute_P<<<dim3(4,9), 256, 0, stream>>>(Wq, bq, Wk, bk, Pnh, Pnl, uB, wB, cB);
-    k_ln0_part<<<dim3(8,25), 256, 0, stream>>>(xy, lnpart);
-    k_ln0_stats<<<1, 64, 0, stream>>>(lnpart, lnstats);
-    k_ln0_apply<<<dim3(25,8), 256, 0, stream>>>(xy, g0, b0, lnstats,
-                                                Vbh, Vbl, Vbth, Vbtl, spartV);
-    k_prep_xyt<<<dim3(25,8), 256, 0, stream>>>(xy, xyTh, xyTl, s2part);
-
-    for (int j = 0; j < 4; ++j) {
-        if (j < 3)
-            k_gemm_g_sym<<<dim3(25,8), 256, 0, stream>>>(Vbth, Vbtl, Gpart);
-        else
-            k_gemm_g_asym<<<dim3(25,8), 256, 0, stream>>>(xyTh, xyTl, Vbth, Vbtl, Gpart);
-        k_gred<<<dim3(8,8), 256, 0, stream>>>(Gpart, wB + j*128, Gbh, Gbl, rpart);
-        k_computeM<<<dim3(2,8), 256, 0, stream>>>(
-            Gbh, Gbl,
-            (j < 3) ? spartV : s2part, (j < 3) ? 100 : 50,
-            Pnh + (size_t)j*16384, Pnl + (size_t)j*16384,
-            uB + j*128, cB + j, rpart, Mth, Mtl, rm);
-        if (j < 3)
-            k_mid<<<dim3(50,8), 256, 0, stream>>>(Vbh, Vbl, Mth, Mtl, rm,
-                                                  gl + j*128, bl + j*128, 1,
-                                                  Vbth, Vbtl, spartV);
-        else
-            k_mid<<<dim3(50,8), 256, 0, stream>>>(Vbh, Vbl, Mth, Mtl, rm,
-                                                  gl, bl, 0,
-                                                  Uth, Utl, spartV);
-    }
-
-    k_gemm_out_mfma<<<dim3(256), 256, 0, stream>>>(W2h, Uth, Utl, out);
-}
+
+    void* kp[] = {
+        (void*)&xy, (void*)&g0, (void*)&b0, (void*)&gl, (void*)&bl,
+        (void*)&lnpart,
+        (void*)&Vbh, (void*)&Vbl, (void*)&Vbth, (void*)&Vbtl,
+        (void*)&xyTh, (void*)&xyTl, (void*)&Uth, (void*)&Utl,
+        (void*)&spartV, (void*)&s2part, (void*)&Gpart,
+        (void*)&Gbh, (void*)&Gbl, (void*)&rpart, (void*)&rm,
+        (void*)&Mth, (void*)&Mtl, (void*)&Pnh, (void*)&Pnl,
+        (void*)&uB, (void*)&wB, (void*)&cB,
+        (void*)&W2h, (void*)&out
+    };
+    hipError_t ce = hipLaunchCooperativeKernel((const void*)k_coop, dim3(256),
+                                               dim3(256), kp, 0, stream);
+    if (ce != hipSuccess) {
+        k_apply_w<<<dim3(400), 256, 0, stream>>>(xy, g0, b0, lnpart,
+                                                 Vbh, Vbl, Vbth, Vbtl,
+                                                 xyTh, xyTl, spartV, s2part);
+        for (int j = 0; j < 4; ++j) {
+            if (j < 3)
+                k_gsym_w<<<dim3(200), 256, 0, stream>>>(Vbth, Vbtl, Gpart);
+            else
+                k_gasym_w<<<dim3(200), 256, 0, stream>>>(xyTh, xyTl, Vbth, Vbtl, Gpart);
+            k_gred_w<<<dim3(64), 256, 0, stream>>>(Gpart, wB + j*128, Gbh, Gbl, rpart);
+            k_cm_w<<<dim3(16), 256, 0, stream>>>(
+                Gbh, Gbl,
+                (j < 3) ? spartV : s2part, (j < 3) ? 100 : 50,
+                Pnh + (size_t)j*16384, Pnl + (size_t)j*16384,
+                uB + j*128, cB + j, rpart, Mth, Mtl, rm);
+            if (j < 3)
+                k_mid_w<<<dim3(400), 256, 0, stream>>>(Vbh, Vbl, Mth, Mtl, rm,
+                                                       gl + j*128, bl + j*128, 1,
+                                                       Vbth, Vbtl, spartV);
+            else
+                k_mid_w<<<dim3(400), 256, 0, stream>>>(Vbh, Vbl, Mth, Mtl, rm,
+                                                       gl, bl, 0,
+                                                       Uth, Utl, spartV);
+        }
+        k_gout_w<<<dim3(200), 256, 0, stream>>>(W2h, Uth, Utl, out);
+    }
+}
```

Result: slower. 1.095 ms (+99.6%).
